# Optimization experiments

Hardware: AMD Instinct MI355X
Metric: run time of the kernel (lower is better)

The kernel has to match this reference:

```python
import jax, jax.numpy as jnp
import numpy as np
import math

H = 512        # hidden_dim
DEPTH = 5
KS = 3         # kernel size
DELTA = 0.1
M = 104        # timestamp == seq_len
NC = 5
B = 512
BN_EPS = 1e-5


def setup_inputs() -> dict:
    key = jax.random.key(0)
    ks = jax.random.split(key, 16)
    inp = {}
    inp['x'] = jax.random.normal(ks[0], (B, 1, M), dtype=jnp.float32)
    # CausalCNN: depth conv layers (first is 1->H, rest H->H), each followed by BN
    inp['conv_w0'] = jax.random.normal(ks[1], (H, 1, KS), dtype=jnp.float32) * (1.0 / np.sqrt(KS))
    inp['conv_b0'] = jnp.zeros((H,), jnp.float32)
    inp['conv_w'] = jax.random.normal(ks[2], (DEPTH - 1, H, H, KS), dtype=jnp.float32) * (1.0 / np.sqrt(H * KS))
    inp['conv_b'] = jnp.zeros((DEPTH - 1, H), jnp.float32)
    inp['bn_gamma'] = jnp.ones((DEPTH, H), jnp.float32)
    inp['bn_beta'] = jnp.zeros((DEPTH, H), jnp.float32)
    # input_proj
    inp['proj_w'] = jax.random.normal(ks[3], (H, H), dtype=jnp.float32) * (1.0 / np.sqrt(H))
    inp['proj_b'] = jnp.zeros((H,), jnp.float32)
    # ZOH layers: A = -0.01*I + 0.001*randn, B = 0.01*randn [H,1], C = 0.01*randn [1,H]
    eye = jnp.eye(H, dtype=jnp.float32)
    inp['A_all'] = -0.01 * eye[None] + 0.001 * jax.random.normal(ks[4], (DEPTH, H, H), dtype=jnp.float32)
    inp['B_all'] = 0.01 * jax.random.normal(ks[5], (DEPTH, H, 1), dtype=jnp.float32)
    inp['C_all'] = 0.01 * jax.random.normal(ks[6], (DEPTH, 1, H), dtype=jnp.float32)
    # fc_temp: Linear(H,H) -> BN1d(H) -> GELU -> Dropout(eval) -> Linear(H,NC)
    inp['fc1_w'] = jax.random.normal(ks[7], (H, H), dtype=jnp.float32) * (1.0 / np.sqrt(H))
    inp['fc1_b'] = jnp.zeros((H,), jnp.float32)
    inp['fc_bn_gamma'] = jnp.ones((H,), jnp.float32)
    inp['fc_bn_beta'] = jnp.zeros((H,), jnp.float32)
    inp['fc2_w'] = jax.random.normal(ks[8], (NC, H), dtype=jnp.float32) * (1.0 / np.sqrt(H))
    inp['fc2_b'] = jnp.zeros((NC,), jnp.float32)
    return inp


def _causal_conv(x, w, b):
    # x: [B, Cin, T], w: [Cout, Cin, K] -> left-pad K-1 (equivalent to pad both + trim right)
    y = jax.lax.conv_general_dilated(x, w, window_strides=(1,), padding=[(KS - 1, 0)],
                                     dimension_numbers=('NCH', 'OIH', 'NCH'))
    return y + b[None, :, None]


def _bn_ct(x, g, b):
    # BatchNorm1d over [B, C, T], batch statistics (training-mode normalization)
    m = x.mean(axis=(0, 2), keepdims=True)
    v = x.var(axis=(0, 2), keepdims=True)
    return g[None, :, None] * (x - m) * jax.lax.rsqrt(v + BN_EPS) + b[None, :, None]


def _pos_encoding(T, d):
    pos = jnp.arange(T, dtype=jnp.float32)[:, None]
    div = jnp.exp(jnp.arange(0, d, 2, dtype=jnp.float32) * (-math.log(10000.0) / d))
    pe = jnp.zeros((T, d), jnp.float32)
    pe = pe.at[:, 0::2].set(jnp.sin(pos * div))
    pe = pe.at[:, 1::2].set(jnp.cos(pos * div))
    return pe


def _zoh_kbar(A, Bv, Cv):
    # A: [H,H], Bv: [H,1], Cv: [1,H] -> normalized K_bar [M]
    A_bar = jax.scipy.linalg.expm(DELTA * A)
    I = jnp.eye(H, dtype=A.dtype)
    A_inv = jnp.linalg.inv(A + 0.001 * I)
    B_bar = A_inv @ (A_bar - I) @ (DELTA * Bv)  # [H,1]
    # term_k = C @ A_bar^k @ B_bar; sequential vector recurrence replaces matrix powers
    def step(v, _):
        term = (Cv @ v)[0, 0]
        return A_bar @ v, term
    _, terms = jax.lax.scan(step, B_bar, None, length=M)  # [M]
    Kb = jnp.flip(terms, axis=0)
    return Kb / (jnp.linalg.norm(Kb) + 1e-6)


def reference(x, conv_w0, conv_b0, conv_w, conv_b, bn_gamma, bn_beta, proj_w, proj_b,
              A_all, B_all, C_all, fc1_w, fc1_b, fc_bn_gamma, fc_bn_beta, fc2_w, fc2_b):
    # CausalCNN
    h = jax.nn.relu(_bn_ct(_causal_conv(x, conv_w0, conv_b0), bn_gamma[0], bn_beta[0]))
    for i in range(DEPTH - 1):
        h = jax.nn.relu(_bn_ct(_causal_conv(h, conv_w[i], conv_b[i]), bn_gamma[i + 1], bn_beta[i + 1]))
    h = jnp.transpose(h, (0, 2, 1))  # [B, T, H]
    # positional encoding + input projection
    h = h + _pos_encoding(M, H)[None]
    h = jnp.einsum('bth,oh->bto', h, proj_w) + proj_b
    # stacked ZOH kernels: each layer multiplies x by its normalized K_bar along time
    Ks = jax.vmap(_zoh_kbar)(A_all, B_all, C_all)  # [DEPTH, M]
    h = h * jnp.prod(Ks, axis=0)[None, :, None]
    # mean pool over time, then fc_temp (BN with batch stats, dropout = identity/eval)
    h = h.mean(axis=1)  # [B, H]
    h = jnp.dot(h, fc1_w.T) + fc1_b
    m = h.mean(axis=0, keepdims=True)
    v = h.var(axis=0, keepdims=True)
    h = fc_bn_gamma * (h - m) * jax.lax.rsqrt(v + BN_EPS) + fc_bn_beta
    h = jax.nn.gelu(h, approximate=False)
    logits = jnp.dot(h, fc2_w.T) + fc2_b  # [B, NC]
    return logits
```

## Files before the change

kernel.cpp:

```cpp
#include <hip/hip_runtime.h>
#include <cstdio>
#include <cmath>
#include <cstdint>

constexpr int BM = 512 * 104;
constexpr float BN_EPS = 1e-5f;

constexpr size_t SZ_BF   = (size_t)BM * 512 * 2;
constexpr size_t SZ_MAT5 = (size_t)5 * 512 * 512 * 4;
constexpr size_t OFF_YB0 = 0;
constexpr size_t OFF_YB1 = OFF_YB0 + SZ_BF;
constexpr size_t OFF_WT2 = OFF_YB1 + SZ_BF;
constexpr size_t OFF_X   = OFF_WT2 + 6291456;
constexpr size_t OFF_T1  = OFF_X   + SZ_MAT5;
constexpr size_t OFF_T2  = OFF_T1  + SZ_MAT5;
constexpr size_t OFF_E   = OFF_T2  + SZ_MAT5;
constexpr size_t OFF_MW  = OFF_E   + SZ_MAT5;
constexpr size_t OFF_P2  = OFF_MW  + SZ_MAT5;
constexpr size_t OFF_P4  = OFF_P2  + SZ_MAT5;
constexpr size_t OFF_ROWT= OFF_P4  + SZ_MAT5;
constexpr size_t OFF_COLS= OFF_ROWT + 655360;
constexpr size_t OFF_COLS2=OFF_COLS + 655360;
constexpr size_t OFF_PIVI= OFF_COLS2 + 655360;
constexpr size_t OFF_PJT = OFF_PIVI + 81920;
constexpr size_t OFF_F1T = OFF_PJT + 1048576;
constexpr size_t OFF_G   = OFF_F1T + 1048576;
constexpr size_t OFF_POOL= OFF_G   + 1048576;
constexpr size_t OFF_Z   = OFF_POOL + 1048576;
constexpr size_t OFF_ST  = OFF_Z   + 1048576;
constexpr size_t OFF_U   = OFF_ST  + 49152;
constexpr size_t OFF_SV  = OFF_U   + 10240;
constexpr size_t OFF_V   = OFF_SV  + 10240;
constexpr size_t OFF_WV  = OFF_V   + 81920;
constexpr size_t OFF_S   = OFF_WV  + 133120;
constexpr size_t WS_NEED = OFF_S + 512;

__device__ __forceinline__ float bf2f(unsigned short u) {
    union { uint32_t i; float f; } x; x.i = (uint32_t)u << 16; return x.f;
}
__device__ __forceinline__ unsigned short f2bf(float f) {
    union { float f; uint32_t i; } x; x.f = f;
    uint32_t r = x.i + 0x7FFFu + ((x.i >> 16) & 1u);
    return (unsigned short)(r >> 16);
}

typedef __bf16 bf16x8 __attribute__((ext_vector_type(8)));
typedef float  f32x4  __attribute__((ext_vector_type(4)));

__device__ __forceinline__ void gld16(const void* g, void* l) {
    __builtin_amdgcn_global_load_lds((const __attribute__((address_space(1))) uint32_t*)g,
                                     (__attribute__((address_space(3))) uint32_t*)l, 16, 0, 0);
}

__global__ void k_build(const float* __restrict__ Aall, float* __restrict__ X, float* __restrict__ MW,
                        float* __restrict__ COLSa, const float* __restrict__ Call, float* __restrict__ WV)
{
    long i = (long)blockIdx.x * 256 + threadIdx.x;
    float a = Aall[i];
    X[i] = 0.1f * a;
    int z = (int)(i >> 18);
    int rc = (int)(i & 262143);
    int r = rc >> 9, c = rc & 511;
    float mw = a + ((r == c) ? 0.001f : 0.0f);
    MW[i] = mw;
    if (c < 64) COLSa[(long)z * 32768 + r * 64 + c] = mw;
    if (i < 2560) WV[(i >> 9) * 6656 + (i & 511)] = Call[i];
}

__global__ __launch_bounds__(256) void k_mm(
    const float* __restrict__ A, long sA, int lda,
    const float* __restrict__ Bm, long sB, int ldb,
    float* __restrict__ C, long sC, int ldc,
    int K, int mode,
    const float* __restrict__ aux, long sAux,
    const float* __restrict__ aux2, float* __restrict__ Cp,
    double* __restrict__ st1, double* __restrict__ st2, int pc)
{
    __shared__ float sm[2 * 32 * 68];
    float* As = sm;
    float* Bs = sm + 32 * 68;
    int z = blockIdx.z;
    A  += (long)z * sA;
    Bm += (long)z * sB;
    C  += (long)z * sC;
    if (aux) aux += (long)z * sAux;
    int m0 = blockIdx.x * 64, n0 = blockIdx.y * 64;
    int tid = threadIdx.x;
    int tx = tid & 15, ty = tid >> 4;
    float acc[4][4] = {};
    for (int k0 = 0; k0 < K; k0 += 32) {
        __syncthreads();
#pragma unroll
        for (int it = 0; it < 2; ++it) {
            int s = it * 256 + tid;
            int mm = s >> 3, k4 = (s & 7) * 4;
            float4 v = *(const float4*)&A[(long)(m0 + mm) * lda + k0 + k4];
            As[(k4 + 0) * 68 + mm] = v.x;
            As[(k4 + 1) * 68 + mm] = v.y;
            As[(k4 + 2) * 68 + mm] = v.z;
            As[(k4 + 3) * 68 + mm] = v.w;
        }
#pragma unroll
        for (int it = 0; it < 2; ++it) {
            int s = it * 256 + tid;
            int kk = s >> 4, n4 = (s & 15) * 4;
            *(float4*)&Bs[kk * 68 + n4] = *(const float4*)&Bm[(long)(k0 + kk) * ldb + n0 + n4];
        }
        __syncthreads();
#pragma unroll 8
        for (int kk = 0; kk < 32; ++kk) {
            float4 a = *(const float4*)&As[kk * 68 + ty * 4];
            float4 b = *(const float4*)&Bs[kk * 68 + tx * 4];
            float av[4] = {a.x, a.y, a.z, a.w};
            float bv[4] = {b.x, b.y, b.z, b.w};
#pragma unroll
            for (int i = 0; i < 4; ++i)
#pragma unroll
                for (int j = 0; j < 4; ++j)
                    acc[i][j] = fmaf(av[i], bv[j], acc[i][j]);
        }
    }
    float sc2 = (mode == 5) ? aux2[0] : 0.0f;
    float cs1[4] = {0, 0, 0, 0}, cs2[4] = {0, 0, 0, 0};
#pragma unroll
    for (int i = 0; i < 4; ++i) {
        int row = m0 + ty * 4 + i;
        int col0 = n0 + tx * 4;
        long base = (long)row * ldc + col0;
        float v[4];
#pragma unroll
        for (int j = 0; j < 4; ++j) v[j] = acc[i][j];
        if (mode == 1) {
            for (int j = 0; j < 4; ++j) {
                int col = col0 + j;
                v[j] = v[j] + 2.0f * aux[(long)row * 512 + col] + ((row == col) ? 1.0f : 0.0f);
            }
        } else if (mode == 2) {
            for (int j = 0; j < 4; ++j)
                v[j] = v[j] + aux[(long)row * 512 + col0 + j];
        } else if (mode == 3) {
            bool inP = (col0 >= pc && col0 < pc + 64);
            if (inP)
                for (int j = 0; j < 4; ++j) v[j] = aux[row * 64 + (col0 + j - pc)];
        } else if (mode == 5) {
            for (int j = 0; j < 4; ++j) v[j] += aux[col0 + j] * sc2;
        } else if (mode == 7) {
            float pv[4];
            for (int j = 0; j < 4; ++j) {
                int col = col0 + j;
                pv[j] = ((row == col) ? 0.5f : 0.0f) + aux[(long)row * 512 + col] * (1.0f / 6.0f)
                        + v[j] * (1.0f / 24.0f);
            }
            *(float4*)&Cp[base] = make_float4(pv[0], pv[1], pv[2], pv[3]);
        } else if (mode == 8) {
            for (int j = 0; j < 4; ++j) {
                v[j] += aux[col0 + j];
                cs1[j] += v[j]; cs2[j] += v[j] * v[j];
            }
        }
        *(float4*)&C[base] = make_float4(v[0], v[1], v[2], v[3]);
    }
    if (mode == 8) {
        __syncthreads();
        float* s1s = sm;
        float* s2s = sm + 1024;
#pragma unroll
        for (int j = 0; j < 4; ++j) {
            s1s[ty * 64 + tx * 4 + j] = cs1[j];
            s2s[ty * 64 + tx * 4 + j] = cs2[j];
        }
        __syncthreads();
        if (tid < 64) {
            double a = 0.0, b = 0.0;
#pragma unroll
            for (int t = 0; t < 16; ++t) { a += s1s[t * 64 + tid]; b += s2s[t * 64 + tid]; }
            atomicAdd(&st1[n0 + tid], a);
            atomicAdd(&st2[n0 + tid], b);
        }
    }
}

__global__ __launch_bounds__(256) void k_elim(
    const float* __restrict__ COLSc, const float* __restrict__ ROWT,
    float* __restrict__ MW, float* __restrict__ COLSn, int pr, int pcn)
{
    int z = blockIdx.z;
    COLSc += (long)z * 32768; ROWT += (long)z * 32768;
    MW += (long)z * 262144; COLSn += (long)z * 32768;
    int m0 = blockIdx.x * 64, n0 = blockIdx.y * 64;
    int tid = threadIdx.x;
    if (m0 == pr) {
        for (int it = 0; it < 16; ++it) {
            int idx = it * 256 + tid;
            int r = idx >> 6, c = idx & 63;
            float v = ROWT[r * 512 + n0 + c];
            MW[(long)(pr + r) * 512 + n0 + c] = v;
            if (n0 == pcn) COLSn[(pr + r) * 64 + c] = v;
        }
        return;
    }
    __shared__ float As[64 * 68];
    __shared__ float Bs[64 * 68];
    {
        int m = tid >> 2, kb = (tid & 3) * 16;
#pragma unroll
        for (int u = 0; u < 4; ++u) {
            float4 v = *(const float4*)&COLSc[(m0 + m) * 64 + kb + u * 4];
            As[(kb + u * 4 + 0) * 68 + m] = v.x;
            As[(kb + u * 4 + 1) * 68 + m] = v.y;
            As[(kb + u * 4 + 2) * 68 + m] = v.z;
            As[(kb + u * 4 + 3) * 68 + m] = v.w;
        }
        int kr = tid >> 2, nb = (tid & 3) * 16;
#pragma unroll
        for (int u = 0; u < 4; ++u)
            *(float4*)&Bs[kr * 68 + nb + u * 4] = *(const float4*)&ROWT[kr * 512 + n0 + nb + u * 4];
    }
    __syncthreads();
    int tx = tid & 15, ty = tid >> 4;
    float acc[4][4] = {};
#pragma unroll 8
    for (int kk = 0; kk < 64; ++kk) {
        float4 a = *(const float4*)&As[kk * 68 + ty * 4];
        float4 b = *(const float4*)&Bs[kk * 68 + tx * 4];
        float av[4] = {a.x, a.y, a.z, a.w};
        float bv[4] = {b.x, b.y, b.z, b.w};
#pragma unroll
        for (int i = 0; i < 4; ++i)
#pragma unroll
            for (int j = 0; j < 4; ++j)
                acc[i][j] = fmaf(av[i], bv[j], acc[i][j]);
    }
    bool inP = (n0 == pr);
#pragma unroll
    for (int i = 0; i < 4; ++i) {
        int row = m0 + ty * 4 + i;
        int col0 = n0 + tx * 4;
        long base = (long)row * 512 + col0;
        float ov[4] = {0.f, 0.f, 0.f, 0.f};
        if (!inP) {
            float4 oldv = *(const float4*)&MW[base];
            ov[0] = oldv.x; ov[1] = oldv.y; ov[2] = oldv.z; ov[3] = oldv.w;
        }
        float v[4];
#pragma unroll
        for (int j = 0; j < 4; ++j) v[j] = ov[j] - acc[i][j];
        *(float4*)&MW[base] = make_float4(v[0], v[1], v[2], v[3]);
        if (n0 == pcn)
            *(float4*)&COLSn[row * 64 + (col0 - pcn)] = make_float4(v[0], v[1], v[2], v[3]);
    }
}

__global__ __launch_bounds__(256) void k_inv64(float* __restrict__ MW, int pblk, float* __restrict__ PIVI)
{
    __shared__ float mat[64 * 65];
    __shared__ float fv[64];
    __shared__ int perm[64];
    __shared__ int arr[64];
    __shared__ int pividx;
    __shared__ float dv;
    int z = blockIdx.x;
    float* Mg = MW + (long)z * 262144 + (long)pblk * 64 * 512 + pblk * 64;
    int tid = threadIdx.x;
    for (int it = 0; it < 16; ++it) {
        int idx = it * 256 + tid;
        int r = idx >> 6, c = idx & 63;
        mat[r * 65 + c] = Mg[r * 512 + c];
    }
    __syncthreads();
    for (int j = 0; j < 64; ++j) {
        if (tid < 64) {
            float v = (tid >= j) ? fabsf(mat[tid * 65 + j]) : -1.0f;
            int idx = tid;
#pragma unroll
            for (int off = 32; off; off >>= 1) {
                float ov = __shfl_down(v, off);
                int oi = __shfl_down(idx, off);
                if (ov > v) { v = ov; idx = oi; }
            }
            if (tid == 0) pividx = idx;
        }
        __syncthreads();
        int r = pividx;
        if (tid < 64) {
            if (r != j) {
                float tj = mat[j * 65 + tid], tr = mat[r * 65 + tid];
                mat[j * 65 + tid] = tr; mat[r * 65 + tid] = tj;
            }
            if (tid == 0) perm[j] = r;
        }
        __syncthreads();
        if (tid < 64) {
            float piv = mat[j * 65 + j];
            float d = 1.0f / piv;
            fv[tid] = mat[tid * 65 + j];
            mat[j * 65 + tid] = (tid == j) ? d : mat[j * 65 + tid] * d;
            if (tid == 0) dv = d;
        }
        __syncthreads();
        {
            int i = tid & 63, c0 = (tid >> 6) * 16;
            if (i != j) {
                float f = fv[i];
                float dd = dv;
#pragma unroll
                for (int u = 0; u < 16; ++u) {
                    int c = c0 + u;
                    float val = mat[i * 65 + c] - f * mat[j * 65 + c];
                    if (c == j) val = -f * dd;
                    mat[i * 65 + c] = val;
                }
            }
        }
        __syncthreads();
    }
    if (tid == 0) {
        for (int c = 0; c < 64; ++c) arr[c] = c;
        for (int j = 63; j >= 0; --j) { int r = perm[j]; int t = arr[j]; arr[j] = arr[r]; arr[r] = t; }
    }
    __syncthreads();
    float* Pg = PIVI + z * 4096;
    for (int it = 0; it < 16; ++it) {
        int idx = it * 256 + tid;
        int r = idx >> 6, c = idx & 63;
        Pg[r * 64 + c] = mat[r * 65 + arr[c]];
    }
}

__global__ void k_matvecA(const float* __restrict__ A, long sA,
                          const float* __restrict__ x, long sx,
                          float* __restrict__ y, long sy,
                          const float* __restrict__ sub, long ssub,
                          float alpha, float beta, int accum)
{
    int row = blockIdx.x, z = blockIdx.y, lane = threadIdx.x;
    A += (long)z * sA; x += (long)z * sx; y += (long)z * sy;
    if (sub) sub += (long)z * ssub;
    const float* ar = A + (long)row * 512;
    double acc = 0.0;
#pragma unroll
    for (int m = 0; m < 8; ++m) {
        int k = lane + m * 64;
        acc += (double)ar[k] * (double)x[k];
    }
    for (int off = 32; off; off >>= 1) acc += __shfl_down(acc, off);
    if (lane == 0) {
        float val = alpha * (float)acc + beta * x[row];
        if (sub) val = sub[row] - val;
        if (accum) y[row] += val; else y[row] = val;
    }
}

struct VWT { long a[8]; long x[8]; long y[8]; float al[8]; float be[8]; int ty[8]; };
__global__ void k_vw(const char* __restrict__ ws, VWT T)
{
    int g = blockIdx.x, z = blockIdx.y, t = blockIdx.z;
    int lane = threadIdx.x;
    const float* A = (const float*)(ws + T.a[t]) + (long)z * 262144;
    int ty = T.ty[t];
    long vs = ty ? 6656 : 4096;
    const float* x = (const float*)(ws + T.x[t]) + (long)z * vs;
    float* yv = (float*)(ws + T.y[t]) + (long)z * vs;
    if (ty == 0) {
        float xm[8];
#pragma unroll
        for (int m = 0; m < 8; ++m) xm[m] = x[lane + m * 64];
        float alpha = T.al[t], beta = T.be[t];
        for (int r0 = 0; r0 < 64; ++r0) {
            int row = g * 64 + r0;
            const float* ar = A + (long)row * 512;
            double acc = 0.0;
#pragma unroll
            for (int m = 0; m < 8; ++m) acc += (double)ar[lane + m * 64] * (double)xm[m];
            for (int off = 32; off; off >>= 1) acc += __shfl_down(acc, off);
            if (lane == 0) yv[row] = alpha * (float)acc + beta * x[row];
        }
    } else {
        __shared__ float xl[512];
#pragma unroll
        for (int m = 0; m < 8; ++m) xl[lane + m * 64] = x[lane + m * 64];
        __syncthreads();
        int c = g * 64 + lane;
        double acc = 0.0;
#pragma unroll 8
        for (int j = 0; j < 512; ++j) acc += (double)A[(long)j * 512 + c] * (double)xl[j];
        yv[c] = (float)acc;
    }
}

__global__ __launch_bounds__(512) void k_termsk(const float* __restrict__ WV, const float* __restrict__ V,
                                                float* __restrict__ svec)
{
    __shared__ float tl[520];
    __shared__ float invn[5];
    __shared__ float red[2];
    int tid = threadIdx.x;
    for (int t = tid; t < 520; t += 512) {
        int z = t / 104, d = t - z * 104;
        int j = d >> 3, i = d & 7;
        const float* wp = WV + z * 6656 + j * 512;
        const float* vp = V + z * 4096 + i * 512;
        float acc = 0.0f;
#pragma unroll 8
        for (int k = 0; k < 512; ++k) acc += wp[k] * vp[k];
        tl[t] = acc;
    }
    __syncthreads();
    int w = tid >> 6, lane = tid & 63;
    if (w < 5) {
        float a = tl[w * 104 + lane]; a = a * a;
        if (lane < 40) { float b = tl[w * 104 + 64 + lane]; a += b * b; }
#pragma unroll
        for (int off = 32; off; off >>= 1) a += __shfl_down(a, off);
        if (lane == 0) invn[w] = 1.0f / (sqrtf(a) + 1e-6f);
    }
    __syncthreads();
    float s = 0.0f;
    if (tid < 104) {
        s = 1.0f;
        for (int l = 0; l < 5; ++l) s *= tl[l * 104 + (103 - tid)] * invn[l];
        svec[tid] = s;
    }
    if (tid < 128) {
        float v = (tid < 104) ? s : 0.0f;
#pragma unroll
        for (int off = 32; off; off >>= 1) v += __shfl_down(v, off);
        if ((tid & 63) == 0) red[tid >> 6] = v;
    }
    __syncthreads();
    if (tid == 0) svec[104] = (red[0] + red[1]) * (1.0f / 104.0f);
}

__global__ void k_conv0(const float* __restrict__ x, const float* __restrict__ w0, const float* __restrict__ b0,
                        unsigned short* __restrict__ y, double* __restrict__ s1g, double* __restrict__ s2g)
{
    int b = blockIdx.x;
    int c = blockIdx.y * 256 + threadIdx.x;
    float w_0 = w0[c * 3 + 0], w_1 = w0[c * 3 + 1], w_2 = w0[c * 3 + 2], bb = b0[c];
    const float* xb = x + b * 104;
    unsigned short* yb = y + (long)b * 104 * 512 + c;
    float xm2 = 0.0f, xm1 = 0.0f;
    float s1 = 0.0f, s2 = 0.0f;
    for (int t = 0; t < 104; ++t) {
        float x0 = xb[t];
        float v = w_0 * xm2 + w_1 * xm1 + w_2 * x0 + bb;
        yb[t * 512] = f2bf(v);
        s1 += v; s2 += v * v;
        xm2 = xm1; xm1 = x0;
    }
    atomicAdd(&s1g[c], (double)s1);
    atomicAdd(&s2g[c], (double)s2);
}

__global__ void k_wt2(const float* __restrict__ W, unsigned short* __restrict__ Wt2)
{
    int co = blockIdx.x, l = blockIdx.y, tid = threadIdx.x;
    const float* src = W + (long)(l * 512 + co) * 512 * 3;
    unsigned short* dst = Wt2 + (long)l * 3 * 262144 + ((long)co << 9);
#pragma unroll
    for (int q = 0; q < 2; ++q) {
        int ci = tid * 2 + q;
        float f0 = src[ci * 3 + 0], f1 = src[ci * 3 + 1], f2 = src[ci * 3 + 2];
        dst[ci] = f2bf(f0);
        dst[262144 + ci] = f2bf(f1);
        dst[524288 + ci] = f2bf(f2);
    }
}

__global__ __launch_bounds__(256) void k_convm(
    const unsigned short* __restrict__ act,
    const unsigned short* __restrict__ Wt2,
    const float* __restrict__ bias,
    const double* __restrict__ STin,
    const float* __restrict__ gam, const float* __restrict__ bet,
    unsigned short* __restrict__ yout,
    double* __restrict__ s1g, double* __restrict__ s2g)
{
    __shared__ __align__(16) unsigned short As[130 * 32];
    __shared__ __align__(16) unsigned short Bs[3 * 128 * 32];
    __shared__ float SCs[512];
    __shared__ float SHs[512];
    int tid = threadIdx.x;
    int m0 = blockIdx.x * 128, co0 = blockIdx.y * 128;
    int w = tid >> 6, lane = tid & 63;
    int wr = (w >> 1) * 64, wc = (w & 1) * 64;
    int fr = lane & 15, fkb = (lane >> 4) * 8, quad = lane >> 4;

    const double invN = 1.0 / (double)BM;
    for (int c = tid; c < 512; c += 256) {
        double mn = STin[c] * invN;
        double var = STin[512 + c] * invN - mn * mn;
        double rs = 1.0 / sqrt(var + (double)BN_EPS);
        double scd = (double)gam[c] * rs;
        SCs[c] = (float)scd;
        SHs[c] = (float)((double)bet[c] - mn * scd);
    }

    bool valid[4][3];
#pragma unroll
    for (int i = 0; i < 4; ++i) {
        int R = m0 + wr + i * 16 + fr;
        int t = R % 104;
#pragma unroll
        for (int tau = 0; tau < 3; ++tau) valid[i][tau] = (t + tau >= 2);
    }
    int ka = (tid & 3) * 8;
    int g0 = m0 - 2 + (tid >> 2); if (g0 < 0) g0 = 0;
    int g1 = m0 + 62 + (tid >> 2);
    int g2 = m0 + 126 + (tid >> 2);
    const unsigned short* pa0 = act + (long)g0 * 512 + ka;
    const unsigned short* pa1 = act + (long)g1 * 512 + ka;
    const unsigned short* pa2 = act + (long)g2 * 512 + ka;
    const unsigned short* pb[6];
#pragma unroll
    for (int it = 0; it < 6; ++it) {
        int c = it * 256 + tid;
        int tau = c >> 9, r = (c >> 2) & 127, kq = (c & 3) * 8;
        pb[it] = Wt2 + ((long)tau << 18) + ((long)(co0 + r) << 9) + kq;
    }

    f32x4 zero4 = {0.f, 0.f, 0.f, 0.f};
    f32x4 acc[4][4];
#pragma unroll
    for (int i = 0; i < 4; ++i)
#pragma unroll
        for (int j = 0; j < 4; ++j) acc[i][j] = zero4;
    bf16x8 zer = {0, 0, 0, 0, 0, 0, 0, 0};

#pragma unroll 1
    for (int s = 0; s < 16; ++s) {
        int ci0 = s * 32;
        int cb = ci0 + ka;
        __syncthreads();
#pragma unroll
        for (int it = 0; it < 6; ++it)
            gld16(pb[it] + ci0, &Bs[it * 2048 + tid * 8]);
        float4 s0 = *(const float4*)&SCs[cb], s1v = *(const float4*)&SCs[cb + 4];
        float4 h0 = *(const float4*)&SHs[cb], h1v = *(const float4*)&SHs[cb + 4];
        float ss[8] = {s0.x, s0.y, s0.z, s0.w, s1v.x, s1v.y, s1v.z, s1v.w};
        float hh[8] = {h0.x, h0.y, h0.z, h0.w, h1v.x, h1v.y, h1v.z, h1v.w};
        int nrep = (tid < 8) ? 3 : 2;
        const unsigned short* pas[3] = {pa0, pa1, pa2};
#pragma unroll
        for (int rep = 0; rep < 3; ++rep) {
            if (rep < nrep) {
                uint4 v = *(const uint4*)(pas[rep] + ci0);
                unsigned short u[8];
                u[0] = (unsigned short)(v.x & 0xFFFF); u[1] = (unsigned short)(v.x >> 16);
                u[2] = (unsigned short)(v.y & 0xFFFF); u[3] = (unsigned short)(v.y >> 16);
                u[4] = (unsigned short)(v.z & 0xFFFF); u[5] = (unsigned short)(v.z >> 16);
                u[6] = (unsigned short)(v.w & 0xFFFF); u[7] = (unsigned short)(v.w >> 16);
                unsigned short o[8];
#pragma unroll
                for (int q = 0; q < 8; ++q)
                    o[q] = f2bf(fmaxf(fmaf(bf2f(u[q]), ss[q], hh[q]), 0.0f));
                uint4 pk;
                pk.x = (uint32_t)o[0] | ((uint32_t)o[1] << 16);
                pk.y = (uint32_t)o[2] | ((uint32_t)o[3] << 16);
                pk.z = (uint32_t)o[4] | ((uint32_t)o[5] << 16);
                pk.w = (uint32_t)o[6] | ((uint32_t)o[7] << 16);
                *(uint4*)&As[rep * 2048 + tid * 8] = pk;
            }
        }
        __syncthreads();
#pragma unroll
        for (int tau = 0; tau < 3; ++tau) {
            bf16x8 af[4], bfr[4];
#pragma unroll
            for (int i = 0; i < 4; ++i) {
                bf16x8 raw = *(const bf16x8*)&As[(wr + i * 16 + fr + tau) * 32 + fkb];
                af[i] = valid[i][tau] ? raw : zer;
            }
#pragma unroll
            for (int j = 0; j < 4; ++j)
                bfr[j] = *(const bf16x8*)&Bs[tau * 4096 + (wc + j * 16 + fr) * 32 + fkb];
#pragma unroll
            for (int i = 0; i < 4; ++i)
#pragma unroll
                for (int j = 0; j < 4; ++j)
                    acc[i][j] = __builtin_amdgcn_mfma_f32_16x16x32_bf16(af[i], bfr[j], acc[i][j], 0, 0, 0);
        }
    }
    float bcol[4], s1[4] = {0, 0, 0, 0}, s2[4] = {0, 0, 0, 0};
#pragma unroll
    for (int jt = 0; jt < 4; ++jt) bcol[jt] = bias[co0 + wc + jt * 16 + fr];
#pragma unroll
    for (int i = 0; i < 4; ++i) {
        int rbase = m0 + wr + i * 16 + quad * 4;
#pragma unroll
        for (int jt = 0; jt < 4; ++jt) {
            int col = co0 + wc + jt * 16 + fr;
#pragma unroll
            for (int r = 0; r < 4; ++r) {
                float v = acc[i][jt][r] + bcol[jt];
                yout[(long)(rbase + r) * 512 + col] = f2bf(v);
                s1[jt] += v; s2[jt] += v * v;
            }
        }
    }
#pragma unroll
    for (int jt = 0; jt < 4; ++jt) {
        s1[jt] += __shfl_xor(s1[jt], 16); s1[jt] += __shfl_xor(s1[jt], 32);
        s2[jt] += __shfl_xor(s2[jt], 16); s2[jt] += __shfl_xor(s2[jt], 32);
    }
    __syncthreads();
    float* st = (float*)As;
    if (lane < 16) {
#pragma unroll
        for (int jt = 0; jt < 4; ++jt) {
            st[w * 64 + jt * 16 + lane] = s1[jt];
            st[256 + w * 64 + jt * 16 + lane] = s2[jt];
        }
    }
    __syncthreads();
    if (tid < 128) {
        int half = tid >> 6, cl = tid & 63;
        float a = st[half * 64 + cl] + st[(half + 2) * 64 + cl];
        float b = st[256 + half * 64 + cl] + st[256 + (half + 2) * 64 + cl];
        atomicAdd(&s1g[co0 + tid], (double)a);
        atomicAdd(&s2g[co0 + tid], (double)b);
    }
}

__global__ void k_pool(const unsigned short* __restrict__ y4, const double* __restrict__ ST4,
                       const float* __restrict__ gam, const float* __restrict__ bet,
                       const float* __restrict__ svec, float* __restrict__ g)
{
    __shared__ float sl[104];
    int b = blockIdx.x;
    int c = blockIdx.y * 256 + threadIdx.x;
    if (threadIdx.x < 104) sl[threadIdx.x] = svec[threadIdx.x];
    __syncthreads();
    const double invN = 1.0 / (double)BM;
    double mn = ST4[c] * invN;
    double var = ST4[512 + c] * invN - mn * mn;
    double rs = 1.0 / sqrt(var + (double)BN_EPS);
    double scd = (double)gam[c] * rs;
    float sc = (float)scd, sh = (float)((double)bet[c] - mn * scd);
    int he = c & ~1;
    float div = expf((float)he * (-0.017988946039015984f));
    float acc = 0.0f;
    const unsigned short* yb = y4 + (long)b * 104 * 512 + c;
    for (int t = 0; t < 104; ++t) {
        float v = bf2f(yb[t * 512]);
        float hn = fmaxf(fmaf(v, sc, sh), 0.0f);
        float arg = (float)t * div;
        float pe = (c & 1) ? cosf(arg) : sinf(arg);
        acc += sl[t] * (hn + pe);
    }
    g[(long)b * 512 + c] = acc * (1.0f / 104.0f);
}

__global__ void k_t512(const float* __restrict__ in0, float* __restrict__ out0,
                       const float* __restrict__ in1, float* __restrict__ out1)
{
    __shared__ float tile[64 * 68];
    const float* in = blockIdx.z ? in1 : in0;
    float* outp = blockIdx.z ? out1 : out0;
    int bx = blockIdx.x, by = blockIdx.y;
    int tid = threadIdx.x;
    for (int it = 0; it < 4; ++it) {
        int s = it * 256 + tid;
        int r = s >> 4, c4 = (s & 15) * 4;
        *(float4*)&tile[r * 68 + c4] = *(const float4*)&in[(long)(bx * 64 + r) * 512 + by * 64 + c4];
    }
    __syncthreads();
    for (int it = 0; it < 4; ++it) {
        int s = it * 256 + tid;
        int r = s >> 4, c4 = (s & 15) * 4;
        float4 v;
        v.x = tile[(c4 + 0) * 68 + r];
        v.y = tile[(c4 + 1) * 68 + r];
        v.z = tile[(c4 + 2) * 68 + r];
        v.w = tile[(c4 + 3) * 68 + r];
        *(float4*)&outp[(long)(by * 64 + r) * 512 + bx * 64 + c4] = v;
    }
}

__global__ __launch_bounds__(256) void k_final(const float* __restrict__ zin, const double* __restrict__ st,
                                               const float* __restrict__ gam, const float* __restrict__ bet,
                                               const float* __restrict__ w2, const float* __restrict__ b2,
                                               float* __restrict__ outp)
{
    __shared__ float red[256];
    int b = blockIdx.x, tid = threadIdx.x;
    int oo[2] = { tid, tid + 256 };
    float gv[2];
#pragma unroll
    for (int q = 0; q < 2; ++q) {
        int o = oo[q];
        double m = st[o] * (1.0 / 512.0);
        double var = st[512 + o] * (1.0 / 512.0) - m * m;
        double rs = 1.0 / sqrt(var + (double)BN_EPS);
        float xn = (float)(((double)zin[(long)b * 512 + o] - m) * rs * (double)gam[o] + (double)bet[o]);
        gv[q] = 0.5f * xn * (1.0f + erff(xn * 0.70710678118654752f));
    }
    for (int n = 0; n < 5; ++n) {
        float p = gv[0] * w2[n * 512 + oo[0]] + gv[1] * w2[n * 512 + oo[1]];
        red[tid] = p;
        __syncthreads();
        for (int off = 128; off; off >>= 1) { if (tid < off) red[tid] += red[tid + off]; __syncthreads(); }
        if (tid == 0) outp[b * 5 + n] = red[0] + b2[n];
        __syncthreads();
    }
}

static void mm(hipStream_t s, int Mt, int Nt, int z,
               const float* A, long sA, int lda,
               const float* B, long sB, int ldb,
               float* C, long sC, int ldc,
               int K, int mode,
               const float* aux = nullptr, long sAux = 0, const float* aux2 = nullptr,
               float* Cp = nullptr, double* st1 = nullptr, double* st2 = nullptr, int pc = 0)
{
    dim3 g(Mt, Nt, z);
    k_mm<<<g, 256, 0, s>>>(A, sA, lda, B, sB, ldb, C, sC, ldc, K, mode, aux, sAux, aux2, Cp, st1, st2, pc);
}

extern "C" void kernel_launch(void* const* d_in, const int* in_sizes, int n_in,
                              void* d_out, int out_size, void* d_ws, size_t ws_size,
                              hipStream_t stream)
{
    (void)in_sizes; (void)n_in; (void)out_size;
    const float* x       = (const float*)d_in[0];
    const float* conv_w0 = (const float*)d_in[1];
    const float* conv_b0 = (const float*)d_in[2];
    const float* conv_w  = (const float*)d_in[3];
    const float* conv_b  = (const float*)d_in[4];
    const float* bn_g    = (const float*)d_in[5];
    const float* bn_b    = (const float*)d_in[6];
    const float* proj_w  = (const float*)d_in[7];
    const float* proj_b  = (const float*)d_in[8];
    const float* A_all   = (const float*)d_in[9];
    const float* B_all   = (const float*)d_in[10];
    const float* C_all   = (const float*)d_in[11];
    const float* fc1_w   = (const float*)d_in[12];
    const float* fc1_b   = (const float*)d_in[13];
    const float* fbn_g   = (const float*)d_in[14];
    const float* fbn_b   = (const float*)d_in[15];
    const float* fc2_w   = (const float*)d_in[16];
    const float* fc2_b   = (const float*)d_in[17];
    float* outp = (float*)d_out;
    char* ws = (char*)d_ws;
    if (ws_size < WS_NEED) { printf("ws too small: %zu < %zu\n", ws_size, WS_NEED); return; }

    unsigned short* YB0 = (unsigned short*)(ws + OFF_YB0);
    unsigned short* YB1 = (unsigned short*)(ws + OFF_YB1);
    unsigned short* WT2 = (unsigned short*)(ws + OFF_WT2);
    float* Xb   = (float*)(ws + OFF_X);
    float* T1   = (float*)(ws + OFF_T1);
    float* T2   = (float*)(ws + OFF_T2);
    float* Eb   = (float*)(ws + OFF_E);
    float* MW   = (float*)(ws + OFF_MW);
    float* P2   = (float*)(ws + OFF_P2);
    float* P4   = (float*)(ws + OFF_P4);
    float* ROWT = (float*)(ws + OFF_ROWT);
    float* COLS1= (float*)(ws + OFF_COLS);
    float* COLS2= (float*)(ws + OFF_COLS2);
    float* PIVI = (float*)(ws + OFF_PIVI);
    float* PJT  = (float*)(ws + OFF_PJT);
    float* F1T  = (float*)(ws + OFF_F1T);
    float* G    = (float*)(ws + OFF_G);
    float* POOL = (float*)(ws + OFF_POOL);
    float* Zb   = (float*)(ws + OFF_Z);
    double* ST  = (double*)(ws + OFF_ST);
    float* U    = (float*)(ws + OFF_U);
    float* SV   = (float*)(ws + OFF_SV);
    float* V    = (float*)(ws + OFF_V);
    float* WV   = (float*)(ws + OFF_WV);
    float* SVEC = (float*)(ws + OFF_S);

    const long SM = 262144;
    hipMemsetAsync(ws + OFF_ST, 0, 49152, stream);

    k_wt2<<<dim3(512, 4), 256, 0, stream>>>(conv_w, WT2);
    k_build<<<5120, 256, 0, stream>>>(A_all, Xb, MW, COLS1, C_all, WV);
    for (int p = 0; p < 8; ++p) {
        int pc = p * 64;
        float* Cc = (p & 1) ? COLS2 : COLS1;
        float* Cn = (p & 1) ? COLS1 : COLS2;
        k_inv64<<<5, 256, 0, stream>>>(MW, p, PIVI);
        mm(stream, 1, 8, 5, PIVI, 4096, 64, MW + pc * 512, SM, 512, ROWT, 32768, 512, 64, 3,
           PIVI, 4096, nullptr, nullptr, nullptr, nullptr, pc);
        k_elim<<<dim3(8, 8, 5), 256, 0, stream>>>(Cc, ROWT, MW, Cn, pc, pc + 64);
    }
    mm(stream, 8, 8, 5, Xb, SM, 512, Xb, SM, 512, T2, SM, 512, 512, 7, Xb, SM, nullptr, T1);
    mm(stream, 8, 8, 5, T2, SM, 512, T1, SM, 512, Eb, SM, 512, 512, 2, Xb, SM);
    mm(stream, 8, 8, 5, Eb, SM, 512, Eb, SM, 512, Xb, SM, 512, 512, 1, Eb, SM);
    mm(stream, 8, 8, 5, Xb, SM, 512, Xb, SM, 512, T1, SM, 512, 512, 0);
    mm(stream, 8, 8, 5, T1, SM, 512, T1, SM, 512, T2, SM, 512, 512, 0);
    mm(stream, 8, 8, 5, T2, SM, 512, T2, SM, 512, P2, SM, 512, 512, 0);
    mm(stream, 8, 8, 5, P2, SM, 512, P2, SM, 512, P4, SM, 512, 512, 0);
    k_matvecA<<<dim3(512, 5), 64, 0, stream>>>(Eb, SM, B_all, 512, U, 512, nullptr, 0, 0.1f, 0.0f, 0);
    k_matvecA<<<dim3(512, 5), 64, 0, stream>>>(MW, SM, U, 512, V, 4096, nullptr, 0, 1.0f, 0.0f, 0);
    k_matvecA<<<dim3(512, 5), 64, 0, stream>>>(A_all, SM, V, 4096, SV, 512, U, 512, 1.0f, 0.001f, 0);
    k_matvecA<<<dim3(512, 5), 64, 0, stream>>>(MW, SM, SV, 512, V, 4096, nullptr, 0, 1.0f, 0.0f, 1);
    auto Voff = [](int i) { return (long)(OFF_V + (size_t)i * 2048); };
    auto Woff = [](int j) { return (long)(OFF_WV + (size_t)j * 2048); };
    {
        VWT T = {};
        T.a[0] = OFF_E;  T.x[0] = Voff(0); T.y[0] = Voff(1); T.al[0] = 1; T.be[0] = 1; T.ty[0] = 0;
        T.a[1] = OFF_T2; T.x[1] = Woff(0); T.y[1] = Woff(1); T.ty[1] = 1;
        k_vw<<<dim3(8, 5, 2), 64, 0, stream>>>(ws, T);
    }
    {
        VWT T = {};
        T.a[0] = OFF_X;  T.x[0] = Voff(0); T.y[0] = Voff(2); T.al[0] = 1; T.ty[0] = 0;
        T.a[1] = OFF_X;  T.x[1] = Voff(1); T.y[1] = Voff(3); T.al[1] = 1; T.ty[1] = 0;
        T.a[2] = OFF_P2; T.x[2] = Woff(0); T.y[2] = Woff(2); T.ty[2] = 1;
        T.a[3] = OFF_P2; T.x[3] = Woff(1); T.y[3] = Woff(3); T.ty[3] = 1;
        k_vw<<<dim3(8, 5, 4), 64, 0, stream>>>(ws, T);
    }
    {
        VWT T = {};
        for (int i = 0; i < 4; ++i) {
            T.a[i] = OFF_T1; T.x[i] = Voff(i); T.y[i] = Voff(4 + i); T.al[i] = 1; T.ty[i] = 0;
            T.a[4 + i] = OFF_P4; T.x[4 + i] = Woff(i); T.y[4 + i] = Woff(4 + i); T.ty[4 + i] = 1;
        }
        k_vw<<<dim3(8, 5, 8), 64, 0, stream>>>(ws, T);
    }
    {
        VWT T = {};
        for (int i = 0; i < 4; ++i) {
            T.a[i] = OFF_P4; T.x[i] = Woff(4 + i); T.y[i] = Woff(8 + i); T.ty[i] = 1;
        }
        k_vw<<<dim3(8, 5, 4), 64, 0, stream>>>(ws, T);
    }
    {
        VWT T = {};
        T.a[0] = OFF_P4; T.x[0] = Woff(8); T.y[0] = Woff(12); T.ty[0] = 1;
        k_vw<<<dim3(8, 5, 1), 64, 0, stream>>>(ws, T);
    }
    k_termsk<<<1, 512, 0, stream>>>(WV, V, SVEC);

    k_conv0<<<dim3(512, 2), 256, 0, stream>>>(x, conv_w0, conv_b0, YB0, ST, ST + 512);
    for (int l = 1; l <= 4; ++l) {
        unsigned short* inb  = (l & 1) ? YB0 : YB1;
        unsigned short* outb = (l & 1) ? YB1 : YB0;
        k_convm<<<dim3(416, 4), 256, 0, stream>>>(inb, WT2 + (size_t)(l - 1) * 3 * 262144,
                                                  conv_b + (l - 1) * 512,
                                                  ST + (l - 1) * 1024, bn_g + (l - 1) * 512, bn_b + (l - 1) * 512,
                                                  outb, ST + l * 1024, ST + l * 1024 + 512);
    }
    k_pool<<<dim3(512, 2), 256, 0, stream>>>(YB0, ST + 4 * 1024, bn_g + 4 * 512, bn_b + 4 * 512, SVEC, G);

    k_t512<<<dim3(8, 8, 2), 256, 0, stream>>>(proj_w, PJT, fc1_w, F1T);
    mm(stream, 8, 8, 1, G, 0, 512, PJT, 0, 512, POOL, 0, 512, 512, 5, proj_b, 0, SVEC + 104);
    mm(stream, 8, 8, 1, POOL, 0, 512, F1T, 0, 512, Zb, 0, 512, 512, 8, fc1_b, 0, nullptr, nullptr,
       ST + 5 * 1024, ST + 5 * 1024 + 512);
    k_final<<<512, 256, 0, stream>>>(Zb, ST + 5 * 1024, fbn_g, fbn_b, fc2_w, fc2_b, outp);
}
```

Before: 1.873 ms.

## Replace matrix exponential squaring chain with batched polynomial and fused block elimination

Replaces the scaling-and-squaring matrix exponential and separate inversion steps with a Taylor power basis (X^1..X^8) computed by batched multi-task GEMM launches, then one elementwise kernel forming several exponential-like combinations. It merges the weight conversion, matrix build and first pivot inversion into one front kernel, reworks block Gaussian elimination into rowscale/elim2 kernels that shrink the grid as pivots advance, and overlays the workspace onto the activation buffer. The conv kernel grid is also halved. This cuts launches and serial GEMM depth but changes numerical approximation (Taylor truncation accuracy) and the conv launch shape.

```diff
diff --git a/kernel.cpp b/kernel.cpp
--- a/kernel.cpp
+++ b/kernel.cpp
@@ -6,34 +6,30 @@
 constexpr int BM = 512 * 104;
 constexpr float BN_EPS = 1e-5f;
 
-constexpr size_t SZ_BF   = (size_t)BM * 512 * 2;
-constexpr size_t SZ_MAT5 = (size_t)5 * 512 * 512 * 4;
-constexpr size_t OFF_YB0 = 0;
-constexpr size_t OFF_YB1 = OFF_YB0 + SZ_BF;
-constexpr size_t OFF_WT2 = OFF_YB1 + SZ_BF;
-constexpr size_t OFF_X   = OFF_WT2 + 6291456;
-constexpr size_t OFF_T1  = OFF_X   + SZ_MAT5;
-constexpr size_t OFF_T2  = OFF_T1  + SZ_MAT5;
-constexpr size_t OFF_E   = OFF_T2  + SZ_MAT5;
-constexpr size_t OFF_MW  = OFF_E   + SZ_MAT5;
-constexpr size_t OFF_P2  = OFF_MW  + SZ_MAT5;
-constexpr size_t OFF_P4  = OFF_P2  + SZ_MAT5;
-constexpr size_t OFF_ROWT= OFF_P4  + SZ_MAT5;
-constexpr size_t OFF_COLS= OFF_ROWT + 655360;
-constexpr size_t OFF_COLS2=OFF_COLS + 655360;
-constexpr size_t OFF_PIVI= OFF_COLS2 + 655360;
-constexpr size_t OFF_PJT = OFF_PIVI + 81920;
-constexpr size_t OFF_F1T = OFF_PJT + 1048576;
-constexpr size_t OFF_G   = OFF_F1T + 1048576;
-constexpr size_t OFF_POOL= OFF_G   + 1048576;
-constexpr size_t OFF_Z   = OFF_POOL + 1048576;
-constexpr size_t OFF_ST  = OFF_Z   + 1048576;
-constexpr size_t OFF_U   = OFF_ST  + 49152;
-constexpr size_t OFF_SV  = OFF_U   + 10240;
-constexpr size_t OFF_V   = OFF_SV  + 10240;
-constexpr size_t OFF_WV  = OFF_V   + 81920;
-constexpr size_t OFF_S   = OFF_WV  + 133120;
-constexpr size_t WS_NEED = OFF_S + 512;
+constexpr size_t SZ_BF = (size_t)BM * 512 * 2;
+constexpr size_t SZ_M5 = (size_t)5 * 512 * 512 * 4;
+constexpr size_t OFF_YB0  = 0;
+constexpr size_t OFF_XP   = 0;
+constexpr size_t OFF_MW   = OFF_XP + 8 * SZ_M5;
+constexpr size_t OFF_ROWT = OFF_MW + SZ_M5;
+constexpr size_t OFF_COLS1= OFF_ROWT + 655360;
+constexpr size_t OFF_COLS2= OFF_COLS1 + 655360;
+constexpr size_t OFF_PIVA = OFF_COLS2 + 655360;
+constexpr size_t OFF_PIVB = OFF_PIVA + 81920;
+constexpr size_t OFF_RU   = OFF_PIVB + 81920;
+static_assert(OFF_RU + 2048 <= SZ_BF, "overlay overflow");
+constexpr size_t OFF_YB1  = SZ_BF;
+constexpr size_t OFF_WT2  = OFF_YB1 + SZ_BF;
+constexpr size_t OFF_PJT  = OFF_WT2 + 6291456;
+constexpr size_t OFF_F1T  = OFF_PJT + 1048576;
+constexpr size_t OFF_G    = OFF_F1T + 1048576;
+constexpr size_t OFF_POOL = OFF_G   + 1048576;
+constexpr size_t OFF_Z    = OFF_POOL + 1048576;
+constexpr size_t OFF_ST   = OFF_Z   + 1048576;
+constexpr size_t OFF_V    = OFF_ST  + 49152;
+constexpr size_t OFF_WV   = OFF_V   + 81920;
+constexpr size_t OFF_SVEC = OFF_WV  + 133120;
+constexpr size_t WS_NEED  = OFF_SVEC + 512;
 
 __device__ __forceinline__ float bf2f(unsigned short u) {
     union { uint32_t i; float f; } x; x.i = (uint32_t)u << 16; return x.f;
@@ -43,7 +39,6 @@
     uint32_t r = x.i + 0x7FFFu + ((x.i >> 16) & 1u);
     return (unsigned short)(r >> 16);
 }
-
 typedef __bf16 bf16x8 __attribute__((ext_vector_type(8)));
 typedef float  f32x4  __attribute__((ext_vector_type(4)));
 
@@ -52,222 +47,13 @@
                                      (__attribute__((address_space(3))) uint32_t*)l, 16, 0, 0);
 }
 
-__global__ void k_build(const float* __restrict__ Aall, float* __restrict__ X, float* __restrict__ MW,
-                        float* __restrict__ COLSa, const float* __restrict__ Call, float* __restrict__ WV)
-{
-    long i = (long)blockIdx.x * 256 + threadIdx.x;
-    float a = Aall[i];
-    X[i] = 0.1f * a;
-    int z = (int)(i >> 18);
-    int rc = (int)(i & 262143);
-    int r = rc >> 9, c = rc & 511;
-    float mw = a + ((r == c) ? 0.001f : 0.0f);
-    MW[i] = mw;
-    if (c < 64) COLSa[(long)z * 32768 + r * 64 + c] = mw;
-    if (i < 2560) WV[(i >> 9) * 6656 + (i & 511)] = Call[i];
-}
-
-__global__ __launch_bounds__(256) void k_mm(
-    const float* __restrict__ A, long sA, int lda,
-    const float* __restrict__ Bm, long sB, int ldb,
-    float* __restrict__ C, long sC, int ldc,
-    int K, int mode,
-    const float* __restrict__ aux, long sAux,
-    const float* __restrict__ aux2, float* __restrict__ Cp,
-    double* __restrict__ st1, double* __restrict__ st2, int pc)
-{
-    __shared__ float sm[2 * 32 * 68];
-    float* As = sm;
-    float* Bs = sm + 32 * 68;
-    int z = blockIdx.z;
-    A  += (long)z * sA;
-    Bm += (long)z * sB;
-    C  += (long)z * sC;
-    if (aux) aux += (long)z * sAux;
-    int m0 = blockIdx.x * 64, n0 = blockIdx.y * 64;
-    int tid = threadIdx.x;
-    int tx = tid & 15, ty = tid >> 4;
-    float acc[4][4] = {};
-    for (int k0 = 0; k0 < K; k0 += 32) {
-        __syncthreads();
-#pragma unroll
-        for (int it = 0; it < 2; ++it) {
-            int s = it * 256 + tid;
-            int mm = s >> 3, k4 = (s & 7) * 4;
-            float4 v = *(const float4*)&A[(long)(m0 + mm) * lda + k0 + k4];
-            As[(k4 + 0) * 68 + mm] = v.x;
-            As[(k4 + 1) * 68 + mm] = v.y;
-            As[(k4 + 2) * 68 + mm] = v.z;
-            As[(k4 + 3) * 68 + mm] = v.w;
-        }
-#pragma unroll
-        for (int it = 0; it < 2; ++it) {
-            int s = it * 256 + tid;
-            int kk = s >> 4, n4 = (s & 15) * 4;
-            *(float4*)&Bs[kk * 68 + n4] = *(const float4*)&Bm[(long)(k0 + kk) * ldb + n0 + n4];
-        }
-        __syncthreads();
-#pragma unroll 8
-        for (int kk = 0; kk < 32; ++kk) {
-            float4 a = *(const float4*)&As[kk * 68 + ty * 4];
-            float4 b = *(const float4*)&Bs[kk * 68 + tx * 4];
-            float av[4] = {a.x, a.y, a.z, a.w};
-            float bv[4] = {b.x, b.y, b.z, b.w};
-#pragma unroll
-            for (int i = 0; i < 4; ++i)
-#pragma unroll
-                for (int j = 0; j < 4; ++j)
-                    acc[i][j] = fmaf(av[i], bv[j], acc[i][j]);
-        }
-    }
-    float sc2 = (mode == 5) ? aux2[0] : 0.0f;
-    float cs1[4] = {0, 0, 0, 0}, cs2[4] = {0, 0, 0, 0};
-#pragma unroll
-    for (int i = 0; i < 4; ++i) {
-        int row = m0 + ty * 4 + i;
-        int col0 = n0 + tx * 4;
-        long base = (long)row * ldc + col0;
-        float v[4];
-#pragma unroll
-        for (int j = 0; j < 4; ++j) v[j] = acc[i][j];
-        if (mode == 1) {
-            for (int j = 0; j < 4; ++j) {
-                int col = col0 + j;
-                v[j] = v[j] + 2.0f * aux[(long)row * 512 + col] + ((row == col) ? 1.0f : 0.0f);
-            }
-        } else if (mode == 2) {
-            for (int j = 0; j < 4; ++j)
-                v[j] = v[j] + aux[(long)row * 512 + col0 + j];
-        } else if (mode == 3) {
-            bool inP = (col0 >= pc && col0 < pc + 64);
-            if (inP)
-                for (int j = 0; j < 4; ++j) v[j] = aux[row * 64 + (col0 + j - pc)];
-        } else if (mode == 5) {
-            for (int j = 0; j < 4; ++j) v[j] += aux[col0 + j] * sc2;
-        } else if (mode == 7) {
-            float pv[4];
-            for (int j = 0; j < 4; ++j) {
-                int col = col0 + j;
-                pv[j] = ((row == col) ? 0.5f : 0.0f) + aux[(long)row * 512 + col] * (1.0f / 6.0f)
-                        + v[j] * (1.0f / 24.0f);
-            }
-            *(float4*)&Cp[base] = make_float4(pv[0], pv[1], pv[2], pv[3]);
-        } else if (mode == 8) {
-            for (int j = 0; j < 4; ++j) {
-                v[j] += aux[col0 + j];
-                cs1[j] += v[j]; cs2[j] += v[j] * v[j];
-            }
-        }
-        *(float4*)&C[base] = make_float4(v[0], v[1], v[2], v[3]);
-    }
-    if (mode == 8) {
-        __syncthreads();
-        float* s1s = sm;
-        float* s2s = sm + 1024;
-#pragma unroll
-        for (int j = 0; j < 4; ++j) {
-            s1s[ty * 64 + tx * 4 + j] = cs1[j];
-            s2s[ty * 64 + tx * 4 + j] = cs2[j];
-        }
-        __syncthreads();
-        if (tid < 64) {
-            double a = 0.0, b = 0.0;
-#pragma unroll
-            for (int t = 0; t < 16; ++t) { a += s1s[t * 64 + tid]; b += s2s[t * 64 + tid]; }
-            atomicAdd(&st1[n0 + tid], a);
-            atomicAdd(&st2[n0 + tid], b);
-        }
-    }
-}
-
-__global__ __launch_bounds__(256) void k_elim(
-    const float* __restrict__ COLSc, const float* __restrict__ ROWT,
-    float* __restrict__ MW, float* __restrict__ COLSn, int pr, int pcn)
-{
-    int z = blockIdx.z;
-    COLSc += (long)z * 32768; ROWT += (long)z * 32768;
-    MW += (long)z * 262144; COLSn += (long)z * 32768;
-    int m0 = blockIdx.x * 64, n0 = blockIdx.y * 64;
-    int tid = threadIdx.x;
-    if (m0 == pr) {
-        for (int it = 0; it < 16; ++it) {
-            int idx = it * 256 + tid;
-            int r = idx >> 6, c = idx & 63;
-            float v = ROWT[r * 512 + n0 + c];
-            MW[(long)(pr + r) * 512 + n0 + c] = v;
-            if (n0 == pcn) COLSn[(pr + r) * 64 + c] = v;
-        }
-        return;
-    }
-    __shared__ float As[64 * 68];
-    __shared__ float Bs[64 * 68];
-    {
-        int m = tid >> 2, kb = (tid & 3) * 16;
-#pragma unroll
-        for (int u = 0; u < 4; ++u) {
-            float4 v = *(const float4*)&COLSc[(m0 + m) * 64 + kb + u * 4];
-            As[(kb + u * 4 + 0) * 68 + m] = v.x;
-            As[(kb + u * 4 + 1) * 68 + m] = v.y;
-            As[(kb + u * 4 + 2) * 68 + m] = v.z;
-            As[(kb + u * 4 + 3) * 68 + m] = v.w;
-        }
-        int kr = tid >> 2, nb = (tid & 3) * 16;
-#pragma unroll
-        for (int u = 0; u < 4; ++u)
-            *(float4*)&Bs[kr * 68 + nb + u * 4] = *(const float4*)&ROWT[kr * 512 + n0 + nb + u * 4];
-    }
-    __syncthreads();
-    int tx = tid & 15, ty = tid >> 4;
-    float acc[4][4] = {};
-#pragma unroll 8
-    for (int kk = 0; kk < 64; ++kk) {
-        float4 a = *(const float4*)&As[kk * 68 + ty * 4];
-        float4 b = *(const float4*)&Bs[kk * 68 + tx * 4];
-        float av[4] = {a.x, a.y, a.z, a.w};
-        float bv[4] = {b.x, b.y, b.z, b.w};
-#pragma unroll
-        for (int i = 0; i < 4; ++i)
-#pragma unroll
-            for (int j = 0; j < 4; ++j)
-                acc[i][j] = fmaf(av[i], bv[j], acc[i][j]);
-    }
-    bool inP = (n0 == pr);
-#pragma unroll
-    for (int i = 0; i < 4; ++i) {
-        int row = m0 + ty * 4 + i;
-        int col0 = n0 + tx * 4;
-        long base = (long)row * 512 + col0;
-        float ov[4] = {0.f, 0.f, 0.f, 0.f};
-        if (!inP) {
-            float4 oldv = *(const float4*)&MW[base];
-            ov[0] = oldv.x; ov[1] = oldv.y; ov[2] = oldv.z; ov[3] = oldv.w;
-        }
-        float v[4];
-#pragma unroll
-        for (int j = 0; j < 4; ++j) v[j] = ov[j] - acc[i][j];
-        *(float4*)&MW[base] = make_float4(v[0], v[1], v[2], v[3]);
-        if (n0 == pcn)
-            *(float4*)&COLSn[row * 64 + (col0 - pcn)] = make_float4(v[0], v[1], v[2], v[3]);
-    }
-}
-
-__global__ __launch_bounds__(256) void k_inv64(float* __restrict__ MW, int pblk, float* __restrict__ PIVI)
-{
-    __shared__ float mat[64 * 65];
-    __shared__ float fv[64];
+__device__ void inv_body(float* mat, float* Pg, int tid)
+{
     __shared__ int perm[64];
     __shared__ int arr[64];
     __shared__ int pividx;
+    __shared__ float fv[64];
     __shared__ float dv;
-    int z = blockIdx.x;
-    float* Mg = MW + (long)z * 262144 + (long)pblk * 64 * 512 + pblk * 64;
-    int tid = threadIdx.x;
-    for (int it = 0; it < 16; ++it) {
-        int idx = it * 256 + tid;
-        int r = idx >> 6, c = idx & 63;
-        mat[r * 65 + c] = Mg[r * 512 + c];
-    }
-    __syncthreads();
     for (int j = 0; j < 64; ++j) {
         if (tid < 64) {
             float v = (tid >= j) ? fabsf(mat[tid * 65 + j]) : -1.0f;
@@ -301,8 +87,7 @@
         {
             int i = tid & 63, c0 = (tid >> 6) * 16;
             if (i != j) {
-                float f = fv[i];
-                float dd = dv;
+                float f = fv[i], dd = dv;
 #pragma unroll
                 for (int u = 0; u < 16; ++u) {
                     int c = c0 + u;
@@ -319,7 +104,6 @@
         for (int j = 63; j >= 0; --j) { int r = perm[j]; int t = arr[j]; arr[j] = arr[r]; arr[r] = t; }
     }
     __syncthreads();
-    float* Pg = PIVI + z * 4096;
     for (int it = 0; it < 16; ++it) {
         int idx = it * 256 + tid;
         int r = idx >> 6, c = idx & 63;
@@ -327,27 +111,293 @@
     }
 }
 
+__global__ __launch_bounds__(256) void k_front(
+    const float* __restrict__ W, unsigned short* __restrict__ Wt2,
+    const float* __restrict__ Aall, float* __restrict__ X, float* __restrict__ MW,
+    float* __restrict__ COLS1, const float* __restrict__ Call, float* __restrict__ WV,
+    float* __restrict__ PIVA)
+{
+    int bid = blockIdx.x, tid = threadIdx.x;
+    if (bid < 2048) {
+        int co = bid & 511, l = bid >> 9;
+        const float* src = W + (long)(l * 512 + co) * 512 * 3;
+        unsigned short* dst = Wt2 + (long)l * 3 * 262144 + ((long)co << 9);
+#pragma unroll
+        for (int q = 0; q < 2; ++q) {
+            int ci = tid * 2 + q;
+            dst[ci]          = f2bf(src[ci * 3 + 0]);
+            dst[262144 + ci] = f2bf(src[ci * 3 + 1]);
+            dst[524288 + ci] = f2bf(src[ci * 3 + 2]);
+        }
+        return;
+    }
+    if (bid < 7168) {
+        long i = (long)(bid - 2048) * 256 + tid;
+        float a = Aall[i];
+        X[i] = 0.1f * a;
+        int z = (int)(i >> 18);
+        int rc = (int)(i & 262143);
+        int r = rc >> 9, c = rc & 511;
+        float mw = a + ((r == c) ? 0.001f : 0.0f);
+        MW[i] = mw;
+        if (c < 64) COLS1[(long)z * 32768 + r * 64 + c] = mw;
+        if (i < 2560) WV[(i >> 9) * 6656 + (i & 511)] = Call[i];
+        return;
+    }
+    {
+        int z = bid - 7168;
+        __shared__ float mat[64 * 65];
+        for (int it = 0; it < 16; ++it) {
+            int idx = it * 256 + tid;
+            int r = idx >> 6, c = idx & 63;
+            mat[r * 65 + c] = Aall[(long)z * 262144 + r * 512 + c] + ((r == c) ? 0.001f : 0.0f);
+        }
+        __syncthreads();
+        inv_body(mat, PIVA + z * 4096, tid);
+    }
+}
+
+struct MMT { long a[4], b[4], c[4]; };
+__global__ __launch_bounds__(256) void k_mmP(const char* __restrict__ ws, MMT T)
+{
+    __shared__ float sm[2 * 32 * 68];
+    float* As = sm;
+    float* Bs = sm + 32 * 68;
+    int task = blockIdx.z / 5, bz = blockIdx.z % 5;
+    const float* A  = (const float*)(ws + T.a[task]) + (long)bz * 262144;
+    const float* Bm = (const float*)(ws + T.b[task]) + (long)bz * 262144;
+    float* C        = (float*)(ws + T.c[task]) + (long)bz * 262144;
+    int m0 = blockIdx.x * 64, n0 = blockIdx.y * 64;
+    int tid = threadIdx.x;
+    int tx = tid & 15, ty = tid >> 4;
+    float acc[4][4] = {};
+    for (int k0 = 0; k0 < 512; k0 += 32) {
+        __syncthreads();
+#pragma unroll
+        for (int it = 0; it < 2; ++it) {
+            int s = it * 256 + tid;
+            int mm = s >> 3, k4 = (s & 7) * 4;
+            float4 v = *(const float4*)&A[(long)(m0 + mm) * 512 + k0 + k4];
+            As[(k4 + 0) * 68 + mm] = v.x;
+            As[(k4 + 1) * 68 + mm] = v.y;
+            As[(k4 + 2) * 68 + mm] = v.z;
+            As[(k4 + 3) * 68 + mm] = v.w;
+        }
+#pragma unroll
+        for (int it = 0; it < 2; ++it) {
+            int s = it * 256 + tid;
+            int kk = s >> 4, n4 = (s & 15) * 4;
+            *(float4*)&Bs[kk * 68 + n4] = *(const float4*)&Bm[(long)(k0 + kk) * 512 + n0 + n4];
+        }
+        __syncthreads();
+#pragma unroll 8
+        for (int kk = 0; kk < 32; ++kk) {
+            float4 a = *(const float4*)&As[kk * 68 + ty * 4];
+            float4 b = *(const float4*)&Bs[kk * 68 + tx * 4];
+            float av[4] = {a.x, a.y, a.z, a.w};
+            float bv[4] = {b.x, b.y, b.z, b.w};
+#pragma unroll
+            for (int i = 0; i < 4; ++i)
+#pragma unroll
+                for (int j = 0; j < 4; ++j)
+                    acc[i][j] = fmaf(av[i], bv[j], acc[i][j]);
+        }
+    }
+#pragma unroll
+    for (int i = 0; i < 4; ++i) {
+        long base = (long)(m0 + ty * 4 + i) * 512 + n0 + tx * 4;
+        *(float4*)&C[base] = make_float4(acc[i][0], acc[i][1], acc[i][2], acc[i][3]);
+    }
+}
+
+struct PolyC { float c[6][8]; };
+__global__ void k_poly(float* __restrict__ XP, PolyC P)
+{
+    long i = (long)blockIdx.x * 256 + threadIdx.x;
+    float x[8];
+#pragma unroll
+    for (int p = 0; p < 8; ++p) x[p] = XP[(long)p * 1310720 + i];
+    float e[6];
+#pragma unroll
+    for (int k = 0; k < 6; ++k) {
+        float s = 0.0f;
+#pragma unroll
+        for (int p = 0; p < 8; ++p) s = fmaf(P.c[k][p], x[p], s);
+        e[k] = s;
+    }
+#pragma unroll
+    for (int k = 0; k < 6; ++k) XP[(long)k * 1310720 + i] = e[k];
+}
+
 __global__ void k_matvecA(const float* __restrict__ A, long sA,
                           const float* __restrict__ x, long sx,
-                          float* __restrict__ y, long sy,
-                          const float* __restrict__ sub, long ssub,
-                          float alpha, float beta, int accum)
+                          float* __restrict__ y, long sy, float alpha)
 {
     int row = blockIdx.x, z = blockIdx.y, lane = threadIdx.x;
     A += (long)z * sA; x += (long)z * sx; y += (long)z * sy;
-    if (sub) sub += (long)z * ssub;
     const float* ar = A + (long)row * 512;
     double acc = 0.0;
 #pragma unroll
-    for (int m = 0; m < 8; ++m) {
-        int k = lane + m * 64;
-        acc += (double)ar[k] * (double)x[k];
-    }
+    for (int m = 0; m < 8; ++m) acc += (double)ar[lane + m * 64] * (double)x[lane + m * 64];
     for (int off = 32; off; off >>= 1) acc += __shfl_down(acc, off);
-    if (lane == 0) {
-        float val = alpha * (float)acc + beta * x[row];
-        if (sub) val = sub[row] - val;
-        if (accum) y[row] += val; else y[row] = val;
+    if (lane == 0) y[row] = alpha * (float)acc;
+}
+
+__global__ __launch_bounds__(256) void k_rowscale(
+    const float* __restrict__ MW, const float* __restrict__ PIVIc,
+    const float* __restrict__ V0, float* __restrict__ ROWT, float* __restrict__ RU, int p)
+{
+    __shared__ float PivT[64 * 68];
+    __shared__ float Bp[64 * 68];
+    __shared__ float uL[64];
+    int z = blockIdx.z, nIdx = blockIdx.x, tid = threadIdx.x;
+    int pr = p * 64;
+    MW += (long)z * 262144; PIVIc += (long)z * 4096; ROWT += (long)z * 32768;
+    for (int it = 0; it < 16; ++it) {
+        int idx = it * 256 + tid;
+        int m = idx >> 6, k = idx & 63;
+        PivT[k * 68 + m] = PIVIc[m * 64 + k];
+    }
+    if (nIdx == 7 - p) {
+        if (tid < 64) uL[tid] = V0[(long)z * 4096 + pr + tid];
+        __syncthreads();
+        if (tid < 64) {
+            float acc = 0.0f;
+            for (int k = 0; k < 64; ++k) acc += PivT[k * 68 + tid] * uL[k];
+            RU[z * 64 + tid] = acc;
+        }
+        return;
+    }
+    int n0 = (p + 1 + nIdx) * 64;
+    {
+        int r = tid >> 2, cb = (tid & 3) * 16;
+#pragma unroll
+        for (int u4 = 0; u4 < 4; ++u4)
+            *(float4*)&Bp[r * 68 + cb + u4 * 4] = *(const float4*)&MW[(long)(pr + r) * 512 + n0 + cb + u4 * 4];
+    }
+    __syncthreads();
+    int tx = tid & 15, ty = tid >> 4;
+    float acc[4][4] = {};
+#pragma unroll 8
+    for (int k = 0; k < 64; ++k) {
+        float4 a = *(const float4*)&PivT[k * 68 + ty * 4];
+        float4 b = *(const float4*)&Bp[k * 68 + tx * 4];
+        float av[4] = {a.x, a.y, a.z, a.w};
+        float bv[4] = {b.x, b.y, b.z, b.w};
+#pragma unroll
+        for (int i = 0; i < 4; ++i)
+#pragma unroll
+            for (int j = 0; j < 4; ++j)
+                acc[i][j] = fmaf(av[i], bv[j], acc[i][j]);
+    }
+#pragma unroll
+    for (int i = 0; i < 4; ++i)
+        *(float4*)&ROWT[(ty * 4 + i) * 512 + n0 + tx * 4] =
+            make_float4(acc[i][0], acc[i][1], acc[i][2], acc[i][3]);
+}
+
+__global__ __launch_bounds__(256) void k_elim2(
+    float* __restrict__ MW, const float* __restrict__ COLSc, float* __restrict__ COLSn,
+    const float* __restrict__ ROWT, const float* __restrict__ RU,
+    float* __restrict__ V0, float* __restrict__ PIVIn, int p)
+{
+    __shared__ float As[64 * 68];
+    __shared__ float Bs[64 * 68];
+    __shared__ float mat[64 * 65];
+    __shared__ float ru[64];
+    int z = blockIdx.z, tid = threadIdx.x;
+    int m0 = blockIdx.x * 64, nIdx = blockIdx.y, pr = p * 64;
+    MW += (long)z * 262144; COLSc += (long)z * 32768; COLSn += (long)z * 32768;
+    ROWT += (long)z * 32768;
+    bool isU = (nIdx == 7 - p);
+    if (isU) {
+        if (m0 == pr) {
+            if (tid < 64) V0[(long)z * 4096 + pr + tid] = RU[z * 64 + tid];
+            return;
+        }
+        if (tid < 64) ru[tid] = RU[z * 64 + tid];
+        {
+            int m = tid >> 2, kb = (tid & 3) * 16;
+#pragma unroll
+            for (int u4 = 0; u4 < 4; ++u4) {
+                float4 v = *(const float4*)&COLSc[(m0 + m) * 64 + kb + u4 * 4];
+                As[(kb + u4 * 4 + 0) * 68 + m] = v.x;
+                As[(kb + u4 * 4 + 1) * 68 + m] = v.y;
+                As[(kb + u4 * 4 + 2) * 68 + m] = v.z;
+                As[(kb + u4 * 4 + 3) * 68 + m] = v.w;
+            }
+        }
+        __syncthreads();
+        if (tid < 64) {
+            float acc = 0.0f;
+            for (int k = 0; k < 64; ++k) acc += As[k * 68 + tid] * ru[k];
+            V0[(long)z * 4096 + m0 + tid] -= acc;
+        }
+        return;
+    }
+    int n0 = (p + 1 + nIdx) * 64;
+    if (m0 == pr) {
+        for (int it = 0; it < 16; ++it) {
+            int idx = it * 256 + tid;
+            int r = idx >> 6, c = idx & 63;
+            float v = ROWT[r * 512 + n0 + c];
+            MW[(long)(pr + r) * 512 + n0 + c] = v;
+            if (n0 == pr + 64) COLSn[(pr + r) * 64 + c] = v;
+        }
+        return;
+    }
+    {
+        int m = tid >> 2, kb = (tid & 3) * 16;
+#pragma unroll
+        for (int u4 = 0; u4 < 4; ++u4) {
+            float4 v = *(const float4*)&COLSc[(m0 + m) * 64 + kb + u4 * 4];
+            As[(kb + u4 * 4 + 0) * 68 + m] = v.x;
+            As[(kb + u4 * 4 + 1) * 68 + m] = v.y;
+            As[(kb + u4 * 4 + 2) * 68 + m] = v.z;
+            As[(kb + u4 * 4 + 3) * 68 + m] = v.w;
+        }
+        int r = tid >> 2, cb = (tid & 3) * 16;
+#pragma unroll
+        for (int u4 = 0; u4 < 4; ++u4)
+            *(float4*)&Bs[r * 68 + cb + u4 * 4] = *(const float4*)&ROWT[r * 512 + n0 + cb + u4 * 4];
+    }
+    __syncthreads();
+    int tx = tid & 15, ty = tid >> 4;
+    float acc[4][4] = {};
+#pragma unroll 8
+    for (int k = 0; k < 64; ++k) {
+        float4 a = *(const float4*)&As[k * 68 + ty * 4];
+        float4 b = *(const float4*)&Bs[k * 68 + tx * 4];
+        float av[4] = {a.x, a.y, a.z, a.w};
+        float bv[4] = {b.x, b.y, b.z, b.w};
+#pragma unroll
+        for (int i = 0; i < 4; ++i)
+#pragma unroll
+            for (int j = 0; j < 4; ++j)
+                acc[i][j] = fmaf(av[i], bv[j], acc[i][j]);
+    }
+    float out[4][4];
+#pragma unroll
+    for (int i = 0; i < 4; ++i) {
+        long base = (long)(m0 + ty * 4 + i) * 512 + n0 + tx * 4;
+        float4 oldv = *(const float4*)&MW[base];
+        out[i][0] = oldv.x - acc[i][0];
+        out[i][1] = oldv.y - acc[i][1];
+        out[i][2] = oldv.z - acc[i][2];
+        out[i][3] = oldv.w - acc[i][3];
+        *(float4*)&MW[base] = make_float4(out[i][0], out[i][1], out[i][2], out[i][3]);
+        if (n0 == pr + 64)
+            *(float4*)&COLSn[(m0 + ty * 4 + i) * 64 + tx * 4] =
+                make_float4(out[i][0], out[i][1], out[i][2], out[i][3]);
+    }
+    if (m0 == pr + 64 && nIdx == 0 && p < 7) {
+#pragma unroll
+        for (int i = 0; i < 4; ++i)
+#pragma unroll
+            for (int j = 0; j < 4; ++j)
+                mat[(ty * 4 + i) * 65 + tx * 4 + j] = out[i][j];
+        __syncthreads();
+        inv_body(mat, PIVIn + (long)z * 4096, tid);
     }
 }
 
@@ -384,7 +434,7 @@
         double acc = 0.0;
 #pragma unroll 8
         for (int j = 0; j < 512; ++j) acc += (double)A[(long)j * 512 + c] * (double)xl[j];
-        yv[c] = (float)acc;
+        yv[c] = (float)acc + T.be[t] * xl[c];
     }
 }
 
@@ -452,22 +502,7 @@
     atomicAdd(&s2g[c], (double)s2);
 }
 
-__global__ void k_wt2(const float* __restrict__ W, unsigned short* __restrict__ Wt2)
-{
-    int co = blockIdx.x, l = blockIdx.y, tid = threadIdx.x;
-    const float* src = W + (long)(l * 512 + co) * 512 * 3;
-    unsigned short* dst = Wt2 + (long)l * 3 * 262144 + ((long)co << 9);
-#pragma unroll
-    for (int q = 0; q < 2; ++q) {
-        int ci = tid * 2 + q;
-        float f0 = src[ci * 3 + 0], f1 = src[ci * 3 + 1], f2 = src[ci * 3 + 2];
-        dst[ci] = f2bf(f0);
-        dst[262144 + ci] = f2bf(f1);
-        dst[524288 + ci] = f2bf(f2);
-    }
-}
-
-__global__ __launch_bounds__(256) void k_convm(
+__global__ __launch_bounds__(256, 1) void k_convm(
     const unsigned short* __restrict__ act,
     const unsigned short* __restrict__ Wt2,
     const float* __restrict__ bias,
@@ -476,14 +511,14 @@
     unsigned short* __restrict__ yout,
     double* __restrict__ s1g, double* __restrict__ s2g)
 {
-    __shared__ __align__(16) unsigned short As[130 * 32];
-    __shared__ __align__(16) unsigned short Bs[3 * 128 * 32];
+    __shared__ __align__(16) unsigned short As[256 * 32];
+    __shared__ __align__(16) unsigned short Bs[256 * 32];
     __shared__ float SCs[512];
     __shared__ float SHs[512];
     int tid = threadIdx.x;
-    int m0 = blockIdx.x * 128, co0 = blockIdx.y * 128;
+    int m0 = blockIdx.x * 256, n0 = blockIdx.y * 256;
     int w = tid >> 6, lane = tid & 63;
-    int wr = (w >> 1) * 64, wc = (w & 1) * 64;
+    int wr = (w >> 1) * 128, wc = (w & 1) * 128;
     int fr = lane & 15, fkb = (lane >> 4) * 8, quad = lane >> 4;
 
     const double invN = 1.0 / (double)BM;
@@ -495,56 +530,38 @@
         SCs[c] = (float)scd;
         SHs[c] = (float)((double)bet[c] - mn * scd);
     }
-
-    bool valid[4][3];
-#pragma unroll
-    for (int i = 0; i < 4; ++i) {
-        int R = m0 + wr + i * 16 + fr;
-        int t = R % 104;
-#pragma unroll
-        for (int tau = 0; tau < 3; ++tau) valid[i][tau] = (t + tau >= 2);
-    }
-    int ka = (tid & 3) * 8;
-    int g0 = m0 - 2 + (tid >> 2); if (g0 < 0) g0 = 0;
-    int g1 = m0 + 62 + (tid >> 2);
-    int g2 = m0 + 126 + (tid >> 2);
-    const unsigned short* pa0 = act + (long)g0 * 512 + ka;
-    const unsigned short* pa1 = act + (long)g1 * 512 + ka;
-    const unsigned short* pa2 = act + (long)g2 * 512 + ka;
-    const unsigned short* pb[6];
-#pragma unroll
-    for (int it = 0; it < 6; ++it) {
-        int c = it * 256 + tid;
-        int tau = c >> 9, r = (c >> 2) & 127, kq = (c & 3) * 8;
-        pb[it] = Wt2 + ((long)tau << 18) + ((long)(co0 + r) << 9) + kq;
-    }
-
-    f32x4 zero4 = {0.f, 0.f, 0.f, 0.f};
-    f32x4 acc[4][4];
-#pragma unroll
-    for (int i = 0; i < 4; ++i)
-#pragma unroll
-        for (int j = 0; j < 4; ++j) acc[i][j] = zero4;
-    bf16x8 zer = {0, 0, 0, 0, 0, 0, 0, 0};
-
+    int arow = tid >> 2, ak = (tid & 3) * 8;
+
+    f32x4 acc[8][8];
+#pragma unroll
+    for (int i = 0; i < 8; ++i)
+#pragma unroll
+        for (int j = 0; j < 8; ++j) { f32x4 zz = {0.f, 0.f, 0.f, 0.f}; acc[i][j] = zz; }
+
+    for (int tau = 0; tau < 3; ++tau) {
 #pragma unroll 1
-    for (int s = 0; s < 16; ++s) {
-        int ci0 = s * 32;
-        int cb = ci0 + ka;
-        __syncthreads();
-#pragma unroll
-        for (int it = 0; it < 6; ++it)
-            gld16(pb[it] + ci0, &Bs[it * 2048 + tid * 8]);
-        float4 s0 = *(const float4*)&SCs[cb], s1v = *(const float4*)&SCs[cb + 4];
-        float4 h0 = *(const float4*)&SHs[cb], h1v = *(const float4*)&SHs[cb + 4];
-        float ss[8] = {s0.x, s0.y, s0.z, s0.w, s1v.x, s1v.y, s1v.z, s1v.w};
-        float hh[8] = {h0.x, h0.y, h0.z, h0.w, h1v.x, h1v.y, h1v.z, h1v.w};
-        int nrep = (tid < 8) ? 3 : 2;
-        const unsigned short* pas[3] = {pa0, pa1, pa2};
-#pragma unroll
-        for (int rep = 0; rep < 3; ++rep) {
-            if (rep < nrep) {
-                uint4 v = *(const uint4*)(pas[rep] + ci0);
+        for (int s = 0; s < 16; ++s) {
+            int ci0 = s * 32;
+            __syncthreads();
+#pragma unroll
+            for (int it = 0; it < 4; ++it) {
+                int q = it * 256 + tid;
+                int co = q >> 2, kq = (q & 3) * 8;
+                gld16(Wt2 + ((long)tau << 18) + ((long)(n0 + co) << 9) + ci0 + kq, &Bs[q * 8]);
+            }
+            int cb = ci0 + ak;
+            float4 s0 = *(const float4*)&SCs[cb], s1v = *(const float4*)&SCs[cb + 4];
+            float4 h0 = *(const float4*)&SHs[cb], h1v = *(const float4*)&SHs[cb + 4];
+            float ss[8] = {s0.x, s0.y, s0.z, s0.w, s1v.x, s1v.y, s1v.z, s1v.w};
+            float hh[8] = {h0.x, h0.y, h0.z, h0.w, h1v.x, h1v.y, h1v.z, h1v.w};
+#pragma unroll
+            for (int it = 0; it < 4; ++it) {
+                int row = it * 64 + arow;
+                int gr = m0 + row;
+                int t = gr % 104;
+                bool val = (t + tau >= 2);
+                uint4 v = make_uint4(0u, 0u, 0u, 0u);
+                if (val) v = *(const uint4*)(act + (long)(gr + tau - 2) * 512 + ci0 + ak);
                 unsigned short u[8];
                 u[0] = (unsigned short)(v.x & 0xFFFF); u[1] = (unsigned short)(v.x >> 16);
                 u[2] = (unsigned short)(v.y & 0xFFFF); u[3] = (unsigned short)(v.y >> 16);
@@ -553,72 +570,70 @@
                 unsigned short o[8];
 #pragma unroll
                 for (int q = 0; q < 8; ++q)
-                    o[q] = f2bf(fmaxf(fmaf(bf2f(u[q]), ss[q], hh[q]), 0.0f));
+                    o[q] = val ? f2bf(fmaxf(fmaf(bf2f(u[q]), ss[q], hh[q]), 0.0f)) : (unsigned short)0;
                 uint4 pk;
                 pk.x = (uint32_t)o[0] | ((uint32_t)o[1] << 16);
                 pk.y = (uint32_t)o[2] | ((uint32_t)o[3] << 16);
                 pk.z = (uint32_t)o[4] | ((uint32_t)o[5] << 16);
                 pk.w = (uint32_t)o[6] | ((uint32_t)o[7] << 16);
-                *(uint4*)&As[rep * 2048 + tid * 8] = pk;
+                *(uint4*)&As[(row << 5) + ak] = pk;
             }
-        }
-        __syncthreads();
-#pragma unroll
-        for (int tau = 0; tau < 3; ++tau) {
-            bf16x8 af[4], bfr[4];
-#pragma unroll
-            for (int i = 0; i < 4; ++i) {
-                bf16x8 raw = *(const bf16x8*)&As[(wr + i * 16 + fr + tau) * 32 + fkb];
-                af[i] = valid[i][tau] ? raw : zer;
+            __syncthreads();
+            bf16x8 af[8], bf[8];
+#pragma unroll
+            for (int i = 0; i < 8; ++i)
+                af[i] = *(const bf16x8*)&As[(wr + i * 16 + fr) * 32 + fkb];
+#pragma unroll
+            for (int j = 0; j < 8; ++j)
+                bf[j] = *(const bf16x8*)&Bs[(wc + j * 16 + fr) * 32 + fkb];
+#pragma unroll
+            for (int i = 0; i < 8; ++i)
+#pragma unroll
+                for (int j = 0; j < 8; ++j)
+                    acc[i][j] = __builtin_amdgcn_mfma_f32_16x16x32_bf16(af[i], bf[j], acc[i][j], 0, 0, 0);
+        }
+    }
+    float bcol[8], s1[8], s2[8];
+#pragma unroll
+    for (int j = 0; j < 8; ++j) {
+        bcol[j] = bias[n0 + wc + j * 16 + fr];
+        s1[j] = 0.f; s2[j] = 0.f;
+    }
+#pragma unroll
+    for (int i = 0; i < 8; ++i) {
+        int rbase = m0 + wr + i * 16 + quad * 4;
+#pragma unroll
+        for (int j = 0; j < 8; ++j) {
+            int col = n0 + wc + j * 16 + fr;
+#pragma unroll
+            for (int r = 0; r < 4; ++r) {
+                float v = acc[i][j][r] + bcol[j];
+                yout[(long)(rbase + r) * 512 + col] = f2bf(v);
+                s1[j] += v; s2[j] += v * v;
             }
-#pragma unroll
-            for (int j = 0; j < 4; ++j)
-                bfr[j] = *(const bf16x8*)&Bs[tau * 4096 + (wc + j * 16 + fr) * 32 + fkb];
-#pragma unroll
-            for (int i = 0; i < 4; ++i)
-#pragma unroll
-                for (int j = 0; j < 4; ++j)
-                    acc[i][j] = __builtin_amdgcn_mfma_f32_16x16x32_bf16(af[i], bfr[j], acc[i][j], 0, 0, 0);
-        }
-    }
-    float bcol[4], s1[4] = {0, 0, 0, 0}, s2[4] = {0, 0, 0, 0};
-#pragma unroll
-    for (int jt = 0; jt < 4; ++jt) bcol[jt] = bias[co0 + wc + jt * 16 + fr];
-#pragma unroll
-    for (int i = 0; i < 4; ++i) {
-        int rbase = m0 + wr + i * 16 + quad * 4;
-#pragma unroll
-        for (int jt = 0; jt < 4; ++jt) {
-            int col = co0 + wc + jt * 16 + fr;
-#pragma unroll
-            for (int r = 0; r < 4; ++r) {
-                float v = acc[i][jt][r] + bcol[jt];
-                yout[(long)(rbase + r) * 512 + col] = f2bf(v);
-                s1[jt] += v; s2[jt] += v * v;
-            }
-        }
-    }
-#pragma unroll
-    for (int jt = 0; jt < 4; ++jt) {
-        s1[jt] += __shfl_xor(s1[jt], 16); s1[jt] += __shfl_xor(s1[jt], 32);
-        s2[jt] += __shfl_xor(s2[jt], 16); s2[jt] += __shfl_xor(s2[jt], 32);
+        }
+    }
+#pragma unroll
+    for (int j = 0; j < 8; ++j) {
+        s1[j] += __shfl_xor(s1[j], 16); s1[j] += __shfl_xor(s1[j], 32);
+        s2[j] += __shfl_xor(s2[j], 16); s2[j] += __shfl_xor(s2[j], 32);
     }
     __syncthreads();
     float* st = (float*)As;
+    int slot = w >> 1;
     if (lane < 16) {
 #pragma unroll
-        for (int jt = 0; jt < 4; ++jt) {
-            st[w * 64 + jt * 16 + lane] = s1[jt];
-            st[256 + w * 64 + jt * 16 + lane] = s2[jt];
+        for (int j = 0; j < 8; ++j) {
+            st[slot * 256 + wc + j * 16 + lane] = s1[j];
+            st[512 + slot * 256 + wc + j * 16 + lane] = s2[j];
         }
     }
     __syncthreads();
-    if (tid < 128) {
-        int half = tid >> 6, cl = tid & 63;
-        float a = st[half * 64 + cl] + st[(half + 2) * 64 + cl];
-        float b = st[256 + half * 64 + cl] + st[256 + (half + 2) * 64 + cl];
-        atomicAdd(&s1g[co0 + tid], (double)a);
-        atomicAdd(&s2g[co0 + tid], (double)b);
+    {
+        float a = st[tid] + st[256 + tid];
+        float b = st[512 + tid] + st[768 + tid];
+        atomicAdd(&s1g[n0 + tid], (double)a);
+        atomicAdd(&s2g[n0 + tid], (double)b);
     }
 }
 
@@ -677,6 +692,89 @@
     }
 }
 
+__global__ __launch_bounds__(256) void k_mm(
+    const float* __restrict__ A, const float* __restrict__ Bm, float* __restrict__ C,
+    int mode, const float* __restrict__ aux, const float* __restrict__ aux2,
+    double* __restrict__ st1, double* __restrict__ st2)
+{
+    __shared__ float sm[2 * 32 * 68];
+    float* As = sm;
+    float* Bs = sm + 32 * 68;
+    int m0 = blockIdx.x * 64, n0 = blockIdx.y * 64;
+    int tid = threadIdx.x;
+    int tx = tid & 15, ty = tid >> 4;
+    float acc[4][4] = {};
+    for (int k0 = 0; k0 < 512; k0 += 32) {
+        __syncthreads();
+#pragma unroll
+        for (int it = 0; it < 2; ++it) {
+            int s = it * 256 + tid;
+            int mm = s >> 3, k4 = (s & 7) * 4;
+            float4 v = *(const float4*)&A[(long)(m0 + mm) * 512 + k0 + k4];
+            As[(k4 + 0) * 68 + mm] = v.x;
+            As[(k4 + 1) * 68 + mm] = v.y;
+            As[(k4 + 2) * 68 + mm] = v.z;
+            As[(k4 + 3) * 68 + mm] = v.w;
+        }
+#pragma unroll
+        for (int it = 0; it < 2; ++it) {
+            int s = it * 256 + tid;
+            int kk = s >> 4, n4 = (s & 15) * 4;
+            *(float4*)&Bs[kk * 68 + n4] = *(const float4*)&Bm[(long)(k0 + kk) * 512 + n0 + n4];
+        }
+        __syncthreads();
+#pragma unroll 8
+        for (int kk = 0; kk < 32; ++kk) {
+            float4 a = *(const float4*)&As[kk * 68 + ty * 4];
+            float4 b = *(const float4*)&Bs[kk * 68 + tx * 4];
+            float av[4] = {a.x, a.y, a.z, a.w};
+            float bv[4] = {b.x, b.y, b.z, b.w};
+#pragma unroll
+            for (int i = 0; i < 4; ++i)
+#pragma unroll
+                for (int j = 0; j < 4; ++j)
+                    acc[i][j] = fmaf(av[i], bv[j], acc[i][j]);
+        }
+    }
+    float sc2 = (mode == 5) ? aux2[0] : 0.0f;
+    float cs1[4] = {0, 0, 0, 0}, cs2[4] = {0, 0, 0, 0};
+#pragma unroll
+    for (int i = 0; i < 4; ++i) {
+        int col0 = n0 + tx * 4;
+        long base = (long)(m0 + ty * 4 + i) * 512 + col0;
+        float v[4];
+#pragma unroll
+        for (int j = 0; j < 4; ++j) v[j] = acc[i][j];
+        if (mode == 5) {
+            for (int j = 0; j < 4; ++j) v[j] += aux[col0 + j] * sc2;
+        } else {
+            for (int j = 0; j < 4; ++j) {
+                v[j] += aux[col0 + j];
+                cs1[j] += v[j]; cs2[j] += v[j] * v[j];
+            }
+        }
+        *(float4*)&C[base] = make_float4(v[0], v[1], v[2], v[3]);
+    }
+    if (mode == 8) {
+        __syncthreads();
+        float* s1s = sm;
+        float* s2s = sm + 1024;
+#pragma unroll
+        for (int j = 0; j < 4; ++j) {
+            s1s[ty * 64 + tx * 4 + j] = cs1[j];
+            s2s[ty * 64 + tx * 4 + j] = cs2[j];
+        }
+        __syncthreads();
+        if (tid < 64) {
+            double a = 0.0, b = 0.0;
+#pragma unroll
+            for (int t = 0; t < 16; ++t) { a += s1s[t * 64 + tid]; b += s2s[t * 64 + tid]; }
+            atomicAdd(&st1[n0 + tid], a);
+            atomicAdd(&st2[n0 + tid], b);
+        }
+    }
+}
+
 __global__ __launch_bounds__(256) void k_final(const float* __restrict__ zin, const double* __restrict__ st,
                                                const float* __restrict__ gam, const float* __restrict__ bet,
                                                const float* __restrict__ w2, const float* __restrict__ b2,
@@ -703,18 +801,6 @@
         if (tid == 0) outp[b * 5 + n] = red[0] + b2[n];
         __syncthreads();
     }
-}
-
-static void mm(hipStream_t s, int Mt, int Nt, int z,
-               const float* A, long sA, int lda,
-               const float* B, long sB, int ldb,
-               float* C, long sC, int ldc,
-               int K, int mode,
-               const float* aux = nullptr, long sAux = 0, const float* aux2 = nullptr,
-               float* Cp = nullptr, double* st1 = nullptr, double* st2 = nullptr, int pc = 0)
-{
-    dim3 g(Mt, Nt, z);
-    k_mm<<<g, 256, 0, s>>>(A, sA, lda, B, sB, ldb, C, sC, ldc, K, mode, aux, sAux, aux2, Cp, st1, st2, pc);
 }
 
 extern "C" void kernel_launch(void* const* d_in, const int* in_sizes, int n_in,
@@ -747,88 +833,101 @@
     unsigned short* YB0 = (unsigned short*)(ws + OFF_YB0);
     unsigned short* YB1 = (unsigned short*)(ws + OFF_YB1);
     unsigned short* WT2 = (unsigned short*)(ws + OFF_WT2);
-    float* Xb   = (float*)(ws + OFF_X);
-    float* T1   = (float*)(ws + OFF_T1);
-    float* T2   = (float*)(ws + OFF_T2);
-    float* Eb   = (float*)(ws + OFF_E);
+    float* XP   = (float*)(ws + OFF_XP);
     float* MW   = (float*)(ws + OFF_MW);
-    float* P2   = (float*)(ws + OFF_P2);
-    float* P4   = (float*)(ws + OFF_P4);
     float* ROWT = (float*)(ws + OFF_ROWT);
-    float* COLS1= (float*)(ws + OFF_COLS);
+    float* COLS1= (float*)(ws + OFF_COLS1);
     float* COLS2= (float*)(ws + OFF_COLS2);
-    float* PIVI = (float*)(ws + OFF_PIVI);
+    float* PIVA = (float*)(ws + OFF_PIVA);
+    float* PIVB = (float*)(ws + OFF_PIVB);
+    float* RU   = (float*)(ws + OFF_RU);
     float* PJT  = (float*)(ws + OFF_PJT);
     float* F1T  = (float*)(ws + OFF_F1T);
     float* G    = (float*)(ws + OFF_G);
     float* POOL = (float*)(ws + OFF_POOL);
     float* Zb   = (float*)(ws + OFF_Z);
     double* ST  = (double*)(ws + OFF_ST);
-    float* U    = (float*)(ws + OFF_U);
-    float* SV   = (float*)(ws + OFF_SV);
     float* V    = (float*)(ws + OFF_V);
     float* WV   = (float*)(ws + OFF_WV);
-    float* SVEC = (float*)(ws + OFF_S);
-
-    const long SM = 262144;
+    float* SVEC = (float*)(ws + OFF_SVEC);
+
     hipMemsetAsync(ws + OFF_ST, 0, 49152, stream);
 
-    k_wt2<<<dim3(512, 4), 256, 0, stream>>>(conv_w, WT2);
-    k_build<<<5120, 256, 0, stream>>>(A_all, Xb, MW, COLS1, C_all, WV);
+    k_front<<<7173, 256, 0, stream>>>(conv_w, WT2, A_all, XP, MW, COLS1, C_all, WV, PIVA);
+
+    auto XPo = [](int p) { return (long)(OFF_XP + (size_t)(p - 1) * SZ_M5); };
+    {
+        MMT T = {};
+        T.a[0] = XPo(1); T.b[0] = XPo(1); T.c[0] = XPo(2);
+        k_mmP<<<dim3(8, 8, 5), 256, 0, stream>>>(ws, T);
+    }
+    {
+        MMT T = {};
+        T.a[0] = XPo(2); T.b[0] = XPo(1); T.c[0] = XPo(3);
+        T.a[1] = XPo(2); T.b[1] = XPo(2); T.c[1] = XPo(4);
+        k_mmP<<<dim3(8, 8, 10), 256, 0, stream>>>(ws, T);
+    }
+    {
+        MMT T = {};
+        T.a[0] = XPo(4); T.b[0] = XPo(1); T.c[0] = XPo(5);
+        T.a[1] = XPo(4); T.b[1] = XPo(2); T.c[1] = XPo(6);
+        T.a[2] = XPo(4); T.b[2] = XPo(3); T.c[2] = XPo(7);
+        T.a[3] = XPo(4); T.b[3] = XPo(4); T.c[3] = XPo(8);
+        k_mmP<<<dim3(8, 8, 20), 256, 0, stream>>>(ws, T);
+    }
+    {
+        PolyC P;
+        for (int k = 0; k < 6; ++k) {
+            double f = (double)(1 << k);
+            double fp = 1.0, fact = 1.0;
+            for (int p = 1; p <= 8; ++p) { fp *= f; fact *= (double)p; P.c[k][p - 1] = (float)(fp / fact); }
+        }
+        k_poly<<<5120, 256, 0, stream>>>(XP, P);
+    }
+    k_matvecA<<<dim3(512, 5), 64, 0, stream>>>(XP, 262144, B_all, 512, V, 4096, 0.1f);
     for (int p = 0; p < 8; ++p) {
-        int pc = p * 64;
-        float* Cc = (p & 1) ? COLS2 : COLS1;
-        float* Cn = (p & 1) ? COLS1 : COLS2;
-        k_inv64<<<5, 256, 0, stream>>>(MW, p, PIVI);
-        mm(stream, 1, 8, 5, PIVI, 4096, 64, MW + pc * 512, SM, 512, ROWT, 32768, 512, 64, 3,
-           PIVI, 4096, nullptr, nullptr, nullptr, nullptr, pc);
-        k_elim<<<dim3(8, 8, 5), 256, 0, stream>>>(Cc, ROWT, MW, Cn, pc, pc + 64);
-    }
-    mm(stream, 8, 8, 5, Xb, SM, 512, Xb, SM, 512, T2, SM, 512, 512, 7, Xb, SM, nullptr, T1);
-    mm(stream, 8, 8, 5, T2, SM, 512, T1, SM, 512, Eb, SM, 512, 512, 2, Xb, SM);
-    mm(stream, 8, 8, 5, Eb, SM, 512, Eb, SM, 512, Xb, SM, 512, 512, 1, Eb, SM);
-    mm(stream, 8, 8, 5, Xb, SM, 512, Xb, SM, 512, T1, SM, 512, 512, 0);
-    mm(stream, 8, 8, 5, T1, SM, 512, T1, SM, 512, T2, SM, 512, 512, 0);
-    mm(stream, 8, 8, 5, T2, SM, 512, T2, SM, 512, P2, SM, 512, 512, 0);
-    mm(stream, 8, 8, 5, P2, SM, 512, P2, SM, 512, P4, SM, 512, 512, 0);
-    k_matvecA<<<dim3(512, 5), 64, 0, stream>>>(Eb, SM, B_all, 512, U, 512, nullptr, 0, 0.1f, 0.0f, 0);
-    k_matvecA<<<dim3(512, 5), 64, 0, stream>>>(MW, SM, U, 512, V, 4096, nullptr, 0, 1.0f, 0.0f, 0);
-    k_matvecA<<<dim3(512, 5), 64, 0, stream>>>(A_all, SM, V, 4096, SV, 512, U, 512, 1.0f, 0.001f, 0);
-    k_matvecA<<<dim3(512, 5), 64, 0, stream>>>(MW, SM, SV, 512, V, 4096, nullptr, 0, 1.0f, 0.0f, 1);
+        const float* Pc = (p & 1) ? PIVB : PIVA;
+        float* Pn       = (p & 1) ? PIVA : PIVB;
+        const float* Cc = (p & 1) ? COLS2 : COLS1;
+        float* Cn       = (p & 1) ? COLS1 : COLS2;
+        k_rowscale<<<dim3(8 - p, 1, 5), 256, 0, stream>>>(MW, Pc, V, ROWT, RU, p);
+        k_elim2<<<dim3(8, 8 - p, 5), 256, 0, stream>>>(MW, Cc, Cn, ROWT, RU, V, Pn, p);
+    }
+    auto Eo = [](int k) { return (long)(OFF_XP + (size_t)k * SZ_M5); };
     auto Voff = [](int i) { return (long)(OFF_V + (size_t)i * 2048); };
     auto Woff = [](int j) { return (long)(OFF_WV + (size_t)j * 2048); };
     {
         VWT T = {};
-        T.a[0] = OFF_E;  T.x[0] = Voff(0); T.y[0] = Voff(1); T.al[0] = 1; T.be[0] = 1; T.ty[0] = 0;
-        T.a[1] = OFF_T2; T.x[1] = Woff(0); T.y[1] = Woff(1); T.ty[1] = 1;
+        T.a[0] = Eo(0); T.x[0] = Voff(0); T.y[0] = Voff(1); T.al[0] = 1; T.be[0] = 1; T.ty[0] = 0;
+        T.a[1] = Eo(3); T.x[1] = Woff(0); T.y[1] = Woff(1); T.be[1] = 1; T.ty[1] = 1;
         k_vw<<<dim3(8, 5, 2), 64, 0, stream>>>(ws, T);
     }
     {
         VWT T = {};
-        T.a[0] = OFF_X;  T.x[0] = Voff(0); T.y[0] = Voff(2); T.al[0] = 1; T.ty[0] = 0;
-        T.a[1] = OFF_X;  T.x[1] = Voff(1); T.y[1] = Voff(3); T.al[1] = 1; T.ty[1] = 0;
-        T.a[2] = OFF_P2; T.x[2] = Woff(0); T.y[2] = Woff(2); T.ty[2] = 1;
-        T.a[3] = OFF_P2; T.x[3] = Woff(1); T.y[3] = Woff(3); T.ty[3] = 1;
+        T.a[0] = Eo(1); T.x[0] = Voff(0); T.y[0] = Voff(2); T.al[0] = 1; T.be[0] = 1; T.ty[0] = 0;
+        T.a[1] = Eo(1); T.x[1] = Voff(1); T.y[1] = Voff(3); T.al[1] = 1; T.be[1] = 1; T.ty[1] = 0;
+        T.a[2] = Eo(4); T.x[2] = Woff(0); T.y[2] = Woff(2); T.be[2] = 1; T.ty[2] = 1;
+        T.a[3] = Eo(4); T.x[3] = Woff(1); T.y[3] = Woff(3); T.be[3] = 1; T.ty[3] = 1;
         k_vw<<<dim3(8, 5, 4), 64, 0, stream>>>(ws, T);
     }
     {
         VWT T = {};
         for (int i = 0; i < 4; ++i) {
-            T.a[i] = OFF_T1; T.x[i] = Voff(i); T.y[i] = Voff(4 + i); T.al[i] = 1; T.ty[i] = 0;
-            T.a[4 + i] = OFF_P4; T.x[4 + i] = Woff(i); T.y[4 + i] = Woff(4 + i); T.ty[4 + i] = 1;
+            T.a[i] = Eo(2); T.x[i] = Voff(i); T.y[i] = Voff(4 + i); T.al[i] = 1; T.be[i] = 1; T.ty[i] = 0;
+            T.a[4 + i] = Eo(5); T.x[4 + i] = Woff(i); T.y[4 + i] = Woff(4 + i); T.be[4 + i] = 1; T.ty[4 + i] = 1;
         }
         k_vw<<<dim3(8, 5, 8), 64, 0, stream>>>(ws, T);
     }
     {
         VWT T = {};
         for (int i = 0; i < 4; ++i) {
-            T.a[i] = OFF_P4; T.x[i] = Woff(4 + i); T.y[i] = Woff(8 + i); T.ty[i] = 1;
+            T.a[i] = Eo(5); T.x[i] = Woff(4 + i); T.y[i] = Woff(8 + i); T.be[i] = 1; T.ty[i] = 1;
         }
         k_vw<<<dim3(8, 5, 4), 64, 0, stream>>>(ws, T);
     }
     {
         VWT T = {};
-        T.a[0] = OFF_P4; T.x[0] = Woff(8); T.y[0] = Woff(12); T.ty[0] = 1;
+        T.a[0] = Eo(5); T.x[0] = Woff(8); T.y[0] = Woff(12); T.be[0] = 1; T.ty[0] = 1;
         k_vw<<<dim3(8, 5, 1), 64, 0, stream>>>(ws, T);
     }
     k_termsk<<<1, 512, 0, stream>>>(WV, V, SVEC);
@@ -837,7 +936,7 @@
     for (int l = 1; l <= 4; ++l) {
         unsigned short* inb  = (l & 1) ? YB0 : YB1;
         unsigned short* outb = (l & 1) ? YB1 : YB0;
-        k_convm<<<dim3(416, 4), 256, 0, stream>>>(inb, WT2 + (size_t)(l - 1) * 3 * 262144,
+        k_convm<<<dim3(208, 2), 256, 0, stream>>>(inb, WT2 + (size_t)(l - 1) * 3 * 262144,
                                                   conv_b + (l - 1) * 512,
                                                   ST + (l - 1) * 1024, bn_g + (l - 1) * 512, bn_b + (l - 1) * 512,
                                                   outb, ST + l * 1024, ST + l * 1024 + 512);
@@ -845,8 +944,7 @@
     k_pool<<<dim3(512, 2), 256, 0, stream>>>(YB0, ST + 4 * 1024, bn_g + 4 * 512, bn_b + 4 * 512, SVEC, G);
 
     k_t512<<<dim3(8, 8, 2), 256, 0, stream>>>(proj_w, PJT, fc1_w, F1T);
-    mm(stream, 8, 8, 1, G, 0, 512, PJT, 0, 512, POOL, 0, 512, 512, 5, proj_b, 0, SVEC + 104);
-    mm(stream, 8, 8, 1, POOL, 0, 512, F1T, 0, 512, Zb, 0, 512, 512, 8, fc1_b, 0, nullptr, nullptr,
-       ST + 5 * 1024, ST + 5 * 1024 + 512);
+    k_mm<<<dim3(8, 8), 256, 0, stream>>>(G, PJT, POOL, 5, proj_b, SVEC + 104, nullptr, nullptr);
+    k_mm<<<dim3(8, 8), 256, 0, stream>>>(POOL, F1T, Zb, 8, fc1_b, nullptr, ST + 5 * 1024, ST + 5 * 1024 + 512);
     k_final<<<512, 256, 0, stream>>>(Zb, ST + 5 * 1024, fbn_g, fbn_b, fc2_w, fc2_b, outp);
 }
```

Result: slower. 2.485 ms (+32.7%).
